# Kernel optimization log

Measured on AMD Instinct MI355X. Metric: run time of the kernel, lower is better.

## Reference

```python
import jax, jax.numpy as jnp
import numpy as np

N_NODES, N_EDGES, BATCH_SIZE = 8192, 65536, 64
N_S, NG, MAX_R = 16, 32, 10.0
SQRT3 = float(np.sqrt(3.0))


def _mlp2(h, w1, b1, w2, b2):
    return jax.nn.relu(h @ w1 + b1) @ w2 + b2


def _mlp3(h, w1, b1, w2, b2, w3, b3):
    h = jax.nn.relu(h @ w1 + b1)
    h = jax.nn.relu(h @ w2 + b2)
    return h @ w3 + b3


def _scatter_mean(vals, idx, n):
    s = jax.ops.segment_sum(vals, idx, num_segments=n)
    c = jax.ops.segment_sum(jnp.ones(vals.shape[:1], vals.dtype), idx, num_segments=n)
    return s / jnp.maximum(c, 1.0)[:, None]


def _forward_molecule(x, pos, src, dst, batch, params):
    (ne_w1, ne_b1, ne_w2, ne_b2, ee_w1, ee_b1, ee_w2, ee_b2,
     c0_w1, c0_b1, c0_w2, c0_b2, c1_w1, c1_b1, c1_w2, c1_b2,
     sn_w1, sn_b1, sn_w2, sn_b2, sn_w3, sn_b3,
     se_w1, se_b1, se_w2, se_b2, se_w3, se_b3) = params
    n = x.shape[0]
    evec = pos[dst] - pos[src]                       # [E,3]
    dist = jnp.sqrt(jnp.sum(evec * evec, -1) + 1e-12)
    mu = jnp.linspace(0.0, MAX_R, NG)
    coeff = -0.5 / (MAX_R / (NG - 1)) ** 2           # GaussianSmearing
    edge_attr = jnp.exp(coeff * (dist[:, None] - mu) ** 2)     # [E,NG]
    sh1 = SQRT3 * evec / dist[:, None]               # l=1 SH, component norm; l=0 part == 1

    h = _mlp2(x, ne_w1, ne_b1, ne_w2, ne_b2)         # node embedding [N,16]
    eemb = _mlp2(edge_attr, ee_w1, ee_b1, ee_w2, ee_b2)        # edge embedding [E,16]

    # ---- conv 0: 16x0e (x) 0e+1o -> 16x0e+16x1o, per-edge TP weights ----
    ea = jnp.concatenate([eemb, h[dst, :N_S], h[src, :N_S]], -1)   # [E,48]
    w = _mlp2(ea, c0_w1, c0_b1, c0_w2, c0_b2)                      # [E,512]
    E = w.shape[0]
    w00 = w[:, :256].reshape(E, 16, 16)    # 0e x 0e -> 0e
    w01 = w[:, 256:].reshape(E, 16, 16)    # 0e x 1o -> 1o
    xs = h[src]
    o0 = 0.25 * jnp.einsum('eu,euw->ew', xs, w00)        # path weight 1/sqrt(16)
    o1 = 0.25 * jnp.einsum('eu,em,euw->ewm', xs, sh1, w01)
    tp = jnp.concatenate([o0, o1.reshape(E, 48)], -1)
    up = _scatter_mean(tp, dst, n)                       # [N,64]
    h = jnp.pad(h, ((0, 0), (0, up.shape[1] - h.shape[1]))) + up

    # ---- conv 1: 16x0e+16x1o (x) 0e+1o -> 16x0e+16x1o+16x1e ----
    ea = jnp.concatenate([eemb, h[dst, :N_S], h[src, :N_S]], -1)
    w = _mlp2(ea, c1_w1, c1_b1, c1_w2, c1_b2)                      # [E,1280]
    wA, wB, wC, wD, wE = (w[:, i * 256:(i + 1) * 256].reshape(E, 16, 16) for i in range(5))
    x0s = h[src, :16]
    x1s = h[src, 16:64].reshape(E, 16, 3)
    pw = 1.0 / float(np.sqrt(32.0))        # two fan-16 paths into 0e and into 1o
    o0 = pw * (jnp.einsum('eu,euw->ew', x0s, wA)
               + jnp.einsum('eui,ei,euw->ew', x1s, sh1, wD) / SQRT3)  # CG(1,1,0)=delta/sqrt3
    o1o = pw * (jnp.einsum('eu,em,euw->ewm', x0s, sh1, wB)
                + jnp.einsum('eum,euw->ewm', x1s, wC))
    cr = jnp.cross(x1s, sh1[:, None, :])                              # CG(1,1,1)=eps/sqrt2
    o1e = (0.25 / float(np.sqrt(2.0))) * jnp.einsum('euk,euw->ewk', cr, wE)
    tp = jnp.concatenate([o0, o1o.reshape(E, 48), o1e.reshape(E, 48)], -1)
    up = _scatter_mean(tp, dst, n)                       # [N,112]
    h = jnp.pad(h, ((0, 0), (0, up.shape[1] - h.shape[1]))) + up

    xf = h[:, :N_S]                                      # n_conv_layers < 3 branch
    s_nodes = _mlp3(xf, sn_w1, sn_b1, sn_w2, sn_b2, sn_w3, sn_b3)   # [N,1]
    s_edges = _mlp3(jnp.concatenate([edge_attr, xf[src], xf[dst]], -1),
                    se_w1, se_b1, se_w2, se_b2, se_w3, se_b3)       # [E,1]
    # edge_in_score=True -> edge and node scatter_add into per-molecule score
    return (jax.ops.segment_sum(s_edges, batch[src], num_segments=BATCH_SIZE)
            + jax.ops.segment_sum(s_nodes, batch, num_segments=BATCH_SIZE))


def setup_inputs() -> dict:
    ks = iter(jax.random.split(jax.random.key(0), 64))

    def nrm(shape, scale=1.0):
        return scale * jax.random.normal(next(ks), shape, jnp.float32)

    def lin(fi, fo):
        return nrm((fi, fo), 1.0 / float(np.sqrt(fi)))

    def z(n):
        return jnp.zeros((n,), jnp.float32)

    inp = {}
    for tag in ('r', 'p'):
        inp[f'x_{tag}'] = nrm((N_NODES, 32))
        inp[f'pos_{tag}'] = 2.0 * jax.random.normal(next(ks), (N_NODES, 3), jnp.float32)
        s = jax.random.randint(next(ks), (N_EDGES,), 0, N_NODES)
        o = jax.random.randint(next(ks), (N_EDGES,), 1, N_NODES)   # no self loops
        inp[f'edge_index_{tag}'] = jnp.stack([s, (s + o) % N_NODES]).astype(jnp.int32)
        inp[f'batch_{tag}'] = jnp.sort(jax.random.randint(next(ks), (N_NODES,), 0, BATCH_SIZE)).astype(jnp.int32)
    inp['ne_w1'] = lin(32, 16); inp['ne_b1'] = z(16); inp['ne_w2'] = lin(16, 16); inp['ne_b2'] = z(16)
    inp['ee_w1'] = lin(32, 16); inp['ee_b1'] = z(16); inp['ee_w2'] = lin(16, 16); inp['ee_b2'] = z(16)
    inp['c0_w1'] = lin(48, 48); inp['c0_b1'] = z(48); inp['c0_w2'] = lin(48, 512); inp['c0_b2'] = z(512)
    inp['c1_w1'] = lin(48, 48); inp['c1_b1'] = z(48); inp['c1_w2'] = lin(48, 1280); inp['c1_b2'] = z(1280)
    inp['sn_w1'] = lin(16, 32); inp['sn_b1'] = z(32); inp['sn_w2'] = lin(32, 16); inp['sn_b2'] = z(16)
    inp['sn_w3'] = lin(16, 1); inp['sn_b3'] = z(1)
    inp['se_w1'] = lin(64, 16); inp['se_b1'] = z(16); inp['se_w2'] = lin(16, 16); inp['se_b2'] = z(16)
    inp['se_w3'] = lin(16, 1); inp['se_b3'] = z(1)
    return inp


def reference(x_r, pos_r, edge_index_r, batch_r, x_p, pos_p, edge_index_p, batch_p,
              ne_w1, ne_b1, ne_w2, ne_b2, ee_w1, ee_b1, ee_w2, ee_b2,
              c0_w1, c0_b1, c0_w2, c0_b2, c1_w1, c1_b1, c1_w2, c1_b2,
              sn_w1, sn_b1, sn_w2, sn_b2, sn_w3, sn_b3,
              se_w1, se_b1, se_w2, se_b2, se_w3, se_b3):
    params = (ne_w1, ne_b1, ne_w2, ne_b2, ee_w1, ee_b1, ee_w2, ee_b2,
              c0_w1, c0_b1, c0_w2, c0_b2, c1_w1, c1_b1, c1_w2, c1_b2,
              sn_w1, sn_b1, sn_w2, sn_b2, sn_w3, sn_b3,
              se_w1, se_b1, se_w2, se_b2, se_w3, se_b3)
    e_r = _forward_molecule(x_r, pos_r, edge_index_r[0], edge_index_r[1], batch_r, params)
    e_p = _forward_molecule(x_p, pos_p, edge_index_p[0], edge_index_p[1], batch_p, params)
    return e_p - e_r   # reaction energy [BATCH_SIZE, 1]
```

## Files before the change

### kernel.cpp

```cpp
#include <hip/hip_runtime.h>
#include <math.h>

#define NN 8192
#define NE 65536
#define SQRT3F 1.7320508075688772f
#define INV_SQRT3F 0.5773502691896258f
#define PW 0.17677669529663687f
#define GSTEP (10.0f/31.0f)
#define GCOEFF (-0.5f/(GSTEP*GSTEP))

typedef _Float16 f16;
typedef f16 f16x2 __attribute__((ext_vector_type(2)));
typedef f16 f16x4 __attribute__((ext_vector_type(4)));
typedef f16 f16x8 __attribute__((ext_vector_type(8)));
typedef float f32x4 __attribute__((ext_vector_type(4)));

#define MFMA(acc, a, b) acc = __builtin_amdgcn_mfma_f32_16x16x32_f16(a, b, acc, 0, 0, 0)

__global__ __launch_bounds__(256) void k_pre(const float* __restrict__ c0w1, const float* __restrict__ c0b1,
                                             const float* __restrict__ c1w1, const float* __restrict__ c1b1,
                                             const float* __restrict__ c0w2, const float* __restrict__ c0b2,
                                             const float* __restrict__ c1w2, const float* __restrict__ c1b2,
                                             f16* __restrict__ w1c0, f16* __restrict__ w1c1,
                                             f16* __restrict__ w2t0, f16* __restrict__ w2t1,
                                             const float* __restrict__ xr, const float* __restrict__ xp,
                                             float* __restrict__ h16f, f16* __restrict__ h16_16,
                                             const float* __restrict__ nw1, const float* __restrict__ nb1,
                                             const float* __restrict__ nw2, const float* __restrict__ nb2,
                                             const int* __restrict__ eir, const int* __restrict__ eip,
                                             const float* __restrict__ posr, const float* __restrict__ posp,
                                             float* __restrict__ sh1d, f16* __restrict__ eemb16,
                                             int* __restrict__ cnt,
                                             const float* __restrict__ ew1, const float* __restrict__ eb1,
                                             const float* __restrict__ ew2, const float* __restrict__ eb2) {
    int b = blockIdx.x;
    int tid = threadIdx.x;
    if (b < 320) {
        int idx = b * 256 + tid;
        if (idx >= 1280 * 64) return;
        int n = idx >> 6, h = idx & 63;
        w2t1[idx] = (f16)((h < 48) ? c1w2[h * 1280 + n] : (h == 48 ? c1b2[n] : 0.f));
        if (n < 512) w2t0[idx] = (f16)((h < 48) ? c0w2[h * 512 + n] : (h == 48 ? c0b2[n] : 0.f));
        if (n < 48) {
            w1c0[idx] = (f16)((h < 48) ? c0w1[h * 48 + n] : (h == 48 ? c0b1[n] : 0.f));
            w1c1[idx] = (f16)((h < 48) ? c1w1[h * 48 + n] : (h == 48 ? c1b1[n] : 0.f));
        }
    } else if (b < 384) {
        int bb = b - 320;
        int mol = bb >> 5;
        const float* x = mol ? xp : xr;
        float* hf = h16f + (size_t)mol * NN * 16;
        f16* h16o = h16_16 + (size_t)mol * NN * 16;
        int v = (bb & 31) * 256 + tid;
        float xi[32];
#pragma unroll
        for (int i = 0; i < 32; i++) xi[i] = x[v * 32 + i];
        float a[16];
#pragma unroll
        for (int j = 0; j < 16; j++) a[j] = nb1[j];
#pragma unroll
        for (int i = 0; i < 32; i++)
#pragma unroll
            for (int j = 0; j < 16; j++) a[j] = fmaf(xi[i], nw1[i * 16 + j], a[j]);
#pragma unroll
        for (int j = 0; j < 16; j++) a[j] = fmaxf(a[j], 0.f);
        float o[16];
#pragma unroll
        for (int j = 0; j < 16; j++) o[j] = nb2[j];
#pragma unroll
        for (int i = 0; i < 16; i++)
#pragma unroll
            for (int j = 0; j < 16; j++) o[j] = fmaf(a[i], nw2[i * 16 + j], o[j]);
#pragma unroll
        for (int j = 0; j < 16; j++) { hf[v * 16 + j] = o[j]; h16o[v * 16 + j] = (f16)o[j]; }
    } else {
        int bb = b - 384;
        int mol = bb >> 8;
        const int* ei = mol ? eip : eir;
        const float* pos = mol ? posp : posr;
        float* sh_ = sh1d + (size_t)mol * NE * 4;
        f16* em_ = eemb16 + (size_t)mol * NE * 16;
        int* cn_ = cnt + mol * NN;
        int e = (bb & 255) * 256 + tid;
        int s = ei[e], d = ei[NE + e];
        float ex = pos[d * 3 + 0] - pos[s * 3 + 0];
        float ey = pos[d * 3 + 1] - pos[s * 3 + 1];
        float ez = pos[d * 3 + 2] - pos[s * 3 + 2];
        float dist = sqrtf(ex * ex + ey * ey + ez * ez + 1e-12f);
        float inv = SQRT3F / dist;
        sh_[e * 4 + 0] = ex * inv;
        sh_[e * 4 + 1] = ey * inv;
        sh_[e * 4 + 2] = ez * inv;
        sh_[e * 4 + 3] = dist;
        float g[32];
#pragma unroll
        for (int i = 0; i < 32; i++) {
            float t = dist - (float)i * GSTEP;
            g[i] = __expf(GCOEFF * t * t);
        }
        float a[16];
#pragma unroll
        for (int j = 0; j < 16; j++) a[j] = eb1[j];
#pragma unroll
        for (int i = 0; i < 32; i++)
#pragma unroll
            for (int j = 0; j < 16; j++) a[j] = fmaf(g[i], ew1[i * 16 + j], a[j]);
#pragma unroll
        for (int j = 0; j < 16; j++) a[j] = fmaxf(a[j], 0.f);
        float o[16];
#pragma unroll
        for (int j = 0; j < 16; j++) o[j] = eb2[j];
#pragma unroll
        for (int i = 0; i < 16; i++)
#pragma unroll
            for (int j = 0; j < 16; j++) o[j] = fmaf(a[i], ew2[i * 16 + j], o[j]);
#pragma unroll
        for (int j = 0; j < 16; j++) em_[e * 16 + j] = (f16)o[j];
        atomicAdd(&cn_[d], 1);
    }
}

__global__ __launch_bounds__(256) void k_scan(int* __restrict__ cnt, int* __restrict__ rowptr,
                                              float* __restrict__ out) {
    __shared__ int part[256];
    int mol = blockIdx.x;
    int* c = cnt + mol * NN;
    int* rp = rowptr + mol * (NN + 1);
    int t = threadIdx.x;
    int base = t * (NN / 256);
    int s = 0;
#pragma unroll
    for (int i = 0; i < NN / 256; i++) s += c[base + i];
    part[t] = s;
    __syncthreads();
    if (t == 0) {
        int run = 0;
        for (int i = 0; i < 256; i++) { int v = part[i]; part[i] = run; run += v; }
    }
    __syncthreads();
    int run = part[t];
    for (int i = 0; i < NN / 256; i++) {
        int cv = c[base + i];
        rp[base + i] = run;
        run += cv;
        c[base + i] = 0;
    }
    if (t == 255) rp[NN] = run;
    if (mol == 0 && t < 64) out[t] = 0.f;
}

__global__ __launch_bounds__(256) void k_fill(const int* __restrict__ eir, const int* __restrict__ eip,
                                              const int* __restrict__ rowptr, int* __restrict__ cnt,
                                              int* __restrict__ eord) {
    int mol = blockIdx.y;
    const int* ei = mol ? eip : eir;
    int e = blockIdx.x * 256 + threadIdx.x;
    int d = ei[NE + e];
    int pos = atomicAdd(&cnt[mol * NN + d], 1);
    eord[mol * NE + rowptr[mol * (NN + 1) + d] + pos] = e;
}

__global__ __launch_bounds__(128) void k_conv0(const int* __restrict__ eir, const int* __restrict__ eip,
                                               const int* __restrict__ eord,
                                               const f16* __restrict__ eemb16, const f16* __restrict__ h16_16,
                                               const float* __restrict__ sh1d,
                                               const f16* __restrict__ w1h, const f16* __restrict__ w2h,
                                               f16* __restrict__ tp0) {
    __shared__ __align__(16) f16 ea[256 * 72];
    __shared__ __align__(16) f16 sc0[256 * 24];
    __shared__ __align__(16) float4 shs[256];
    int mol = blockIdx.y;
    const int* ei = mol ? eip : eir;
    const int* eo = eord + mol * NE;
    const f16* em_ = eemb16 + (size_t)mol * NE * 16;
    const f16* h16_ = h16_16 + (size_t)mol * NN * 16;
    const float* sh_ = sh1d + (size_t)mol * NE * 4;
    f16* tp_ = tp0 + (size_t)mol * NE * 64;
    int tid = threadIdx.x;
    int e0 = blockIdx.x * 256;
#pragma unroll
    for (int ii = 0; ii < 2; ii++) {
        int er = tid * 2 + ii;
        int le = eo[e0 + er];
        int s = ei[le], d = ei[NE + le];
        char* row = (char*)ea + er * 144;
        const f16x8* pe = (const f16x8*)(em_ + (size_t)le * 16);
        ((f16x8*)row)[0] = pe[0]; ((f16x8*)row)[1] = pe[1];
        const f16x8* pd = (const f16x8*)(h16_ + (size_t)d * 16);
        ((f16x8*)row)[2] = pd[0]; ((f16x8*)row)[3] = pd[1];
        const f16x8* ps = (const f16x8*)(h16_ + (size_t)s * 16);
        f16x8 sv0 = ps[0], sv1 = ps[1];
        ((f16x8*)row)[4] = sv0; ((f16x8*)row)[5] = sv1;
        f16x8 z = {}; f16x8 o = {}; o[0] = (f16)1.0f;
        ((f16x8*)row)[6] = o; ((f16x8*)row)[7] = z; ((f16x8*)row)[8] = z;
        char* srow = (char*)sc0 + er * 48;
        *(f16x8*)srow = sv0;
        *(f16x8*)(srow + 16) = sv1;
        shs[er] = *(const float4*)(sh_ + (size_t)le * 4);
    }
    int wv = tid >> 6, l = tid & 63;
    int koff = (l >> 4) * 16;
    int voffB = (l & 15) * 128 + koff;
    int rbase = wv * 128;
#pragma unroll
    for (int t = 0; t < 8; t++) {
        int arow = rbase + t * 16 + (l & 15);
        f16x8 a0 = *(const f16x8*)((const char*)ea + arow * 144 + koff);
        f16x8 a1 = *(const f16x8*)((const char*)ea + arow * 144 + koff + 64);
#pragma unroll
        for (int nt = 0; nt < 3; nt++) {
            f32x4 hacc = {0.f, 0.f, 0.f, 0.f};
            const char* hb = (const char*)w1h + nt * 2048 + voffB;
            MFMA(hacc, a0, *(const f16x8*)(hb));
            MFMA(hacc, a1, *(const f16x8*)(hb + 64));
#pragma unroll
            for (int r = 0; r < 4; r++) {
                int rr = rbase + t * 16 + (l >> 4) * 4 + r;
                ea[rr * 72 + nt * 16 + (l & 15)] = (f16)fmaxf(hacc[r], 0.f);
            }
        }
    }
    f16x8 ha0[8], ha1[8];
#pragma unroll
    for (int t = 0; t < 8; t++) {
        int arow = rbase + t * 16 + (l & 15);
        ha0[t] = *(const f16x8*)((const char*)ea + arow * 144 + koff);
        ha1[t] = *(const f16x8*)((const char*)ea + arow * 144 + koff + 64);
    }
    f32x4 accA[8] = {}, accB[8] = {};
    const char* wB = (const char*)w2h + voffB;
    f16x8 cA0 = *(const f16x8*)(wB), cA1 = *(const f16x8*)(wB + 64);
    f16x8 cB0 = *(const f16x8*)(wB + 32768), cB1 = *(const f16x8*)(wB + 32768 + 64);
#pragma unroll 4
    for (int u = 0; u < 16; ++u) {
        int un = (u < 15) ? u + 1 : 15;
        const char* Hb = wB + un * 2048;
        f16x8 nA0 = *(const f16x8*)(Hb), nA1 = *(const f16x8*)(Hb + 64);
        f16x8 nB0 = *(const f16x8*)(Hb + 32768), nB1 = *(const f16x8*)(Hb + 32768 + 64);
#pragma unroll
        for (int t = 0; t < 8; t++) {
            f16 s = *(const f16*)((const char*)sc0 + (rbase + t * 16 + (l & 15)) * 48 + u * 2);
            f16x8 x0 = ha0[t] * s, x1 = ha1[t] * s;
            MFMA(accA[t], x0, cA0); MFMA(accA[t], x1, cA1);
            MFMA(accB[t], x0, cB0); MFMA(accB[t], x1, cB1);
        }
        cA0 = nA0; cA1 = nA1; cB0 = nB0; cB1 = nB1;
    }
    int w = l & 15;
#pragma unroll
    for (int t = 0; t < 8; t++)
#pragma unroll
        for (int r = 0; r < 4; r++) {
            int ro = rbase + t * 16 + (l >> 4) * 4 + r;
            int i = e0 + ro;
            float4 shv = shs[ro];
            f16* tpp = tp_ + (size_t)i * 64;
            float tb = 0.25f * accB[t][r];
            tpp[w] = (f16)(0.25f * accA[t][r]);
            tpp[16 + w] = (f16)(tb * shv.x);
            tpp[32 + w] = (f16)(tb * shv.y);
            tpp[48 + w] = (f16)(tb * shv.z);
        }
}

__global__ __launch_bounds__(256) void k_up0g(const float* __restrict__ h16f, const f16* __restrict__ tp0,
                                              const int* __restrict__ rowptr,
                                              float* __restrict__ h64f, f16* __restrict__ h64_16) {
    int mol = blockIdx.y;
    const float* h_ = h16f + (size_t)mol * NN * 16;
    const f16* tp = tp0 + (size_t)mol * NE * 64;
    const int* rp = rowptr + mol * (NN + 1);
    float* o_ = h64f + (size_t)mol * NN * 64;
    f16* o16_ = h64_16 + (size_t)mol * NN * 16;
    int tid = threadIdx.x;
    int v = blockIdx.x * 64 + (tid >> 2), q = tid & 3;
    int r0 = rp[v], r1 = rp[v + 1];
    float acc[16];
#pragma unroll
    for (int j = 0; j < 16; j++) acc[j] = 0.f;
    for (int i = r0; i < r1; i++) {
        const f16* src = tp + (size_t)i * 64 + q * 16;
        f16x8 v0 = *(const f16x8*)src;
        f16x8 v1 = *(const f16x8*)(src + 8);
#pragma unroll
        for (int j = 0; j < 8; j++) { acc[j] += (float)v0[j]; acc[8 + j] += (float)v1[j]; }
    }
    float rc = 1.0f / fmaxf((float)(r1 - r0), 1.0f);
    if (q == 0) {
#pragma unroll
        for (int w = 0; w < 16; w++) {
            float val = fmaf(acc[w], rc, h_[(size_t)v * 16 + w]);
            o_[(size_t)v * 64 + w] = val;
            o16_[(size_t)v * 16 + w] = (f16)val;
        }
    } else {
#pragma unroll
        for (int w = 0; w < 16; w++) o_[(size_t)v * 64 + 16 + 3 * w + (q - 1)] = acc[w] * rc;
    }
}

__global__ __launch_bounds__(128) void k_conv1(const int* __restrict__ eir, const int* __restrict__ eip,
                                               const int* __restrict__ eord,
                                               const f16* __restrict__ eemb16, const f16* __restrict__ h64_16,
                                               const float* __restrict__ h64f, const float* __restrict__ sh1d,
                                               const f16* __restrict__ w1h, const f16* __restrict__ w2h,
                                               f16* __restrict__ tp1) {
    __shared__ __align__(16) f16 ea[256 * 72];
    __shared__ __align__(16) f16 sc1[256 * 36];
    int mol = blockIdx.y;
    const int* ei = mol ? eip : eir;
    const int* eo = eord + mol * NE;
    const f16* em_ = eemb16 + (size_t)mol * NE * 16;
    const f16* h16_ = h64_16 + (size_t)mol * NN * 16;
    const float* hf_ = h64f + (size_t)mol * NN * 64;
    const float* sh_ = sh1d + (size_t)mol * NE * 4;
    f16* tp_ = tp1 + (size_t)mol * NE * 16;
    int tid = threadIdx.x;
    int e0 = blockIdx.x * 256;
#pragma unroll
    for (int ii = 0; ii < 2; ii++) {
        int er = tid * 2 + ii;
        int le = eo[e0 + er];
        int s = ei[le], d = ei[NE + le];
        char* row = (char*)ea + er * 144;
        const f16x8* pe = (const f16x8*)(em_ + (size_t)le * 16);
        ((f16x8*)row)[0] = pe[0]; ((f16x8*)row)[1] = pe[1];
        const f16x8* pd = (const f16x8*)(h16_ + (size_t)d * 16);
        ((f16x8*)row)[2] = pd[0]; ((f16x8*)row)[3] = pd[1];
        const f16x8* ps = (const f16x8*)(h16_ + (size_t)s * 16);
        ((f16x8*)row)[4] = ps[0]; ((f16x8*)row)[5] = ps[1];
        f16x8 z = {}; f16x8 o = {}; o[0] = (f16)1.0f;
        ((f16x8*)row)[6] = o; ((f16x8*)row)[7] = z; ((f16x8*)row)[8] = z;
        float4 shv = *(const float4*)(sh_ + (size_t)le * 4);
        const float* hfs = hf_ + (size_t)s * 64;
        float xu[16];
#pragma unroll
        for (int g = 0; g < 4; g++) {
            float4 v4 = *(const float4*)(hfs + g * 4);
            xu[g * 4 + 0] = v4.x; xu[g * 4 + 1] = v4.y; xu[g * 4 + 2] = v4.z; xu[g * 4 + 3] = v4.w;
        }
        float x1v[48];
#pragma unroll
        for (int g = 0; g < 12; g++) {
            float4 v4 = *(const float4*)(hfs + 16 + g * 4);
            x1v[g * 4 + 0] = v4.x; x1v[g * 4 + 1] = v4.y; x1v[g * 4 + 2] = v4.z; x1v[g * 4 + 3] = v4.w;
        }
        char* srow = (char*)sc1 + er * 72;
#pragma unroll
        for (int g = 0; g < 4; g++) {
            f16x8 pk;
#pragma unroll
            for (int k2 = 0; k2 < 4; k2++) {
                int k = g * 4 + k2;
                float du = (x1v[k * 3] * shv.x + x1v[k * 3 + 1] * shv.y + x1v[k * 3 + 2] * shv.z) * INV_SQRT3F;
                pk[k2 * 2 + 0] = (f16)xu[k];
                pk[k2 * 2 + 1] = (f16)du;
            }
            *(f16x8*)(srow + g * 16) = pk;
        }
    }
    int wv = tid >> 6, l = tid & 63;
    int koff = (l >> 4) * 16;
    int voffB = (l & 15) * 128 + koff;
    int rbase = wv * 128;
#pragma unroll
    for (int t = 0; t < 8; t++) {
        int arow = rbase + t * 16 + (l & 15);
        f16x8 a0 = *(const f16x8*)((const char*)ea + arow * 144 + koff);
        f16x8 a1 = *(const f16x8*)((const char*)ea + arow * 144 + koff + 64);
#pragma unroll
        for (int nt = 0; nt < 3; nt++) {
            f32x4 hacc = {0.f, 0.f, 0.f, 0.f};
            const char* hb = (const char*)w1h + nt * 2048 + voffB;
            MFMA(hacc, a0, *(const f16x8*)(hb));
            MFMA(hacc, a1, *(const f16x8*)(hb + 64));
#pragma unroll
            for (int r = 0; r < 4; r++) {
                int rr = rbase + t * 16 + (l >> 4) * 4 + r;
                ea[rr * 72 + nt * 16 + (l & 15)] = (f16)fmaxf(hacc[r], 0.f);
            }
        }
    }
    f16x8 ha0[8], ha1[8];
#pragma unroll
    for (int t = 0; t < 8; t++) {
        int arow = rbase + t * 16 + (l & 15);
        ha0[t] = *(const f16x8*)((const char*)ea + arow * 144 + koff);
        ha1[t] = *(const f16x8*)((const char*)ea + arow * 144 + koff + 64);
    }
    f32x4 accA[8] = {};
    const char* wB = (const char*)w2h + voffB;
    f16x8 cA0 = *(const f16x8*)(wB), cA1 = *(const f16x8*)(wB + 64);
    f16x8 cD0 = *(const f16x8*)(wB + 98304), cD1 = *(const f16x8*)(wB + 98304 + 64);
#pragma unroll 4
    for (int u = 0; u < 16; ++u) {
        int un = (u < 15) ? u + 1 : 15;
        const char* Hb = wB + un * 2048;
        f16x8 nA0 = *(const f16x8*)(Hb), nA1 = *(const f16x8*)(Hb + 64);
        f16x8 nD0 = *(const f16x8*)(Hb + 98304), nD1 = *(const f16x8*)(Hb + 98304 + 64);
#pragma unroll
        for (int t = 0; t < 8; t++) {
            f16x2 sp = *(const f16x2*)((const char*)sc1 + (rbase + t * 16 + (l & 15)) * 72 + u * 4);
            f16x8 x0 = ha0[t] * sp[0], x1 = ha1[t] * sp[0];
            MFMA(accA[t], x0, cA0); MFMA(accA[t], x1, cA1);
            x0 = ha0[t] * sp[1]; x1 = ha1[t] * sp[1];
            MFMA(accA[t], x0, cD0); MFMA(accA[t], x1, cD1);
        }
        cA0 = nA0; cA1 = nA1; cD0 = nD0; cD1 = nD1;
    }
    int w = l & 15;
#pragma unroll
    for (int t = 0; t < 8; t++)
#pragma unroll
        for (int r = 0; r < 4; r++) {
            int i = e0 + rbase + t * 16 + (l >> 4) * 4 + r;
            tp_[(size_t)i * 16 + w] = (f16)(PW * accA[t][r]);
        }
}

__global__ __launch_bounds__(256) void k_xfg(const float* __restrict__ h64f, const f16* __restrict__ tp1,
                                             const int* __restrict__ rowptr,
                                             float* __restrict__ xf,
                                             const int* __restrict__ batchr, const int* __restrict__ batchp,
                                             const float* __restrict__ w1, const float* __restrict__ b1,
                                             const float* __restrict__ w2, const float* __restrict__ b2,
                                             const float* __restrict__ w3, const float* __restrict__ b3,
                                             float* __restrict__ out) {
    __shared__ float xfs[64][17];
    __shared__ float buck[64];
    int tid = threadIdx.x;
    if (tid < 64) buck[tid] = 0.f;
    int mol = blockIdx.y;
    float sign = mol ? 1.f : -1.f;
    const int* batch = mol ? batchp : batchr;
    const float* h_ = h64f + (size_t)mol * NN * 64;
    const f16* tp = tp1 + (size_t)mol * NE * 16;
    const int* rp = rowptr + mol * (NN + 1);
    float* xf_ = xf + (size_t)mol * NN * 16;
    int v = blockIdx.x * 64 + (tid >> 2), q = tid & 3;
    int r0 = rp[v], r1 = rp[v + 1];
    float a0 = 0.f, a1 = 0.f, a2 = 0.f, a3 = 0.f;
    for (int i = r0; i < r1; i++) {
        f16x4 t4 = *(const f16x4*)(tp + (size_t)i * 16 + q * 4);
        a0 += (float)t4[0]; a1 += (float)t4[1]; a2 += (float)t4[2]; a3 += (float)t4[3];
    }
    float rc = 1.0f / fmaxf((float)(r1 - r0), 1.0f);
    float4 hv = *(const float4*)(h_ + (size_t)v * 64 + q * 4);
    float4 xv4;
    xv4.x = fmaf(a0, rc, hv.x); xv4.y = fmaf(a1, rc, hv.y);
    xv4.z = fmaf(a2, rc, hv.z); xv4.w = fmaf(a3, rc, hv.w);
    xfs[tid >> 2][q * 4 + 0] = xv4.x; xfs[tid >> 2][q * 4 + 1] = xv4.y;
    xfs[tid >> 2][q * 4 + 2] = xv4.z; xfs[tid >> 2][q * 4 + 3] = xv4.w;
    *(float4*)(xf_ + (size_t)v * 16 + q * 4) = xv4;
    __syncthreads();
    if (tid < 64) {
        int v2 = blockIdx.x * 64 + tid;
        float xv[16];
#pragma unroll
        for (int c = 0; c < 16; c++) xv[c] = xfs[tid][c];
        float aa[32];
#pragma unroll
        for (int j = 0; j < 32; j++) aa[j] = b1[j];
#pragma unroll
        for (int i = 0; i < 16; i++)
#pragma unroll
            for (int j = 0; j < 32; j++) aa[j] = fmaf(xv[i], w1[i * 32 + j], aa[j]);
#pragma unroll
        for (int j = 0; j < 32; j++) aa[j] = fmaxf(aa[j], 0.f);
        float bb[16];
#pragma unroll
        for (int j = 0; j < 16; j++) bb[j] = b2[j];
#pragma unroll
        for (int i = 0; i < 32; i++)
#pragma unroll
            for (int j = 0; j < 16; j++) bb[j] = fmaf(aa[i], w2[i * 16 + j], bb[j]);
#pragma unroll
        for (int j = 0; j < 16; j++) bb[j] = fmaxf(bb[j], 0.f);
        float val = b3[0];
#pragma unroll
        for (int i = 0; i < 16; i++) val = fmaf(bb[i], w3[i], val);
        atomicAdd(&buck[batch[v2]], val);
    }
    __syncthreads();
    if (tid < 64) atomicAdd(&out[tid], sign * buck[tid]);
}

__global__ __launch_bounds__(256) void k_sedge(const int* __restrict__ eir, const int* __restrict__ eip,
                                               const int* __restrict__ batchr, const int* __restrict__ batchp,
                                               const float* __restrict__ sh1d, const float* __restrict__ xf,
                                               const float* __restrict__ w1, const float* __restrict__ b1,
                                               const float* __restrict__ w2, const float* __restrict__ b2,
                                               const float* __restrict__ w3, const float* __restrict__ b3,
                                               float* __restrict__ out) {
    __shared__ float buck[64];
    int tid = threadIdx.x;
    if (tid < 64) buck[tid] = 0.f;
    __syncthreads();
    int mol = blockIdx.y;
    float sign = mol ? 1.f : -1.f;
    const int* ei = mol ? eip : eir;
    const int* batch = mol ? batchp : batchr;
    const float* sh_ = sh1d + (size_t)mol * NE * 4;
    const float* xf_ = xf + (size_t)mol * NN * 16;
    int e = blockIdx.x * 256 + tid;
    int s = ei[e], d = ei[NE + e];
    float dist = sh_[e * 4 + 3];
    float in[64];
#pragma unroll
    for (int i = 0; i < 32; i++) {
        float t = dist - (float)i * GSTEP;
        in[i] = __expf(GCOEFF * t * t);
    }
#pragma unroll
    for (int i = 0; i < 16; i++) in[32 + i] = xf_[s * 16 + i];
#pragma unroll
    for (int i = 0; i < 16; i++) in[48 + i] = xf_[d * 16 + i];
    float a[16];
#pragma unroll
    for (int j = 0; j < 16; j++) a[j] = b1[j];
#pragma unroll
    for (int i = 0; i < 64; i++)
#pragma unroll
        for (int j = 0; j < 16; j++) a[j] = fmaf(in[i], w1[i * 16 + j], a[j]);
#pragma unroll
    for (int j = 0; j < 16; j++) a[j] = fmaxf(a[j], 0.f);
    float bb[16];
#pragma unroll
    for (int j = 0; j < 16; j++) bb[j] = b2[j];
#pragma unroll
    for (int i = 0; i < 16; i++)
#pragma unroll
        for (int j = 0; j < 16; j++) bb[j] = fmaf(a[i], w2[i * 16 + j], bb[j]);
#pragma unroll
    for (int j = 0; j < 16; j++) bb[j] = fmaxf(bb[j], 0.f);
    float val = b3[0];
#pragma unroll
    for (int i = 0; i < 16; i++) val = fmaf(bb[i], w3[i], val);
    atomicAdd(&buck[batch[s]], val);
    __syncthreads();
    if (tid < 64) atomicAdd(&out[tid], sign * buck[tid]);
}

extern "C" void kernel_launch(void* const* d_in, const int* in_sizes, int n_in,
                              void* d_out, int out_size, void* d_ws, size_t ws_size,
                              hipStream_t stream) {
    const float* x_r = (const float*)d_in[0];
    const float* pos_r = (const float*)d_in[1];
    const int* ei_r = (const int*)d_in[2];
    const int* batch_r = (const int*)d_in[3];
    const float* x_p = (const float*)d_in[4];
    const float* pos_p = (const float*)d_in[5];
    const int* ei_p = (const int*)d_in[6];
    const int* batch_p = (const int*)d_in[7];
    const float* ne_w1 = (const float*)d_in[8];
    const float* ne_b1 = (const float*)d_in[9];
    const float* ne_w2 = (const float*)d_in[10];
    const float* ne_b2 = (const float*)d_in[11];
    const float* ee_w1 = (const float*)d_in[12];
    const float* ee_b1 = (const float*)d_in[13];
    const float* ee_w2 = (const float*)d_in[14];
    const float* ee_b2 = (const float*)d_in[15];
    const float* c0_w1 = (const float*)d_in[16];
    const float* c0_b1 = (const float*)d_in[17];
    const float* c0_w2 = (const float*)d_in[18];
    const float* c0_b2 = (const float*)d_in[19];
    const float* c1_w1 = (const float*)d_in[20];
    const float* c1_b1 = (const float*)d_in[21];
    const float* c1_w2 = (const float*)d_in[22];
    const float* c1_b2 = (const float*)d_in[23];
    const float* sn_w1 = (const float*)d_in[24];
    const float* sn_b1 = (const float*)d_in[25];
    const float* sn_w2 = (const float*)d_in[26];
    const float* sn_b2 = (const float*)d_in[27];
    const float* sn_w3 = (const float*)d_in[28];
    const float* sn_b3 = (const float*)d_in[29];
    const float* se_w1 = (const float*)d_in[30];
    const float* se_b1 = (const float*)d_in[31];
    const float* se_w2 = (const float*)d_in[32];
    const float* se_b2 = (const float*)d_in[33];
    const float* se_w3 = (const float*)d_in[34];
    const float* se_b3 = (const float*)d_in[35];
    float* out = (float*)d_out;

    char* p = (char*)d_ws;
    auto alloc = [&](size_t bytes) { char* r = p; p += (bytes + 255) & ~(size_t)255; return r; };
    f16* w2t1 = (f16*)alloc(1280 * 64 * 2);
    f16* w2t0 = (f16*)alloc(512 * 64 * 2);
    f16* w1c0 = (f16*)alloc(48 * 64 * 2);
    f16* w1c1 = (f16*)alloc(48 * 64 * 2);
    f16* eemb16 = (f16*)alloc((size_t)2 * NE * 16 * 2);
    f16* h16_16 = (f16*)alloc((size_t)2 * NN * 16 * 2);
    f16* h64_16 = (f16*)alloc((size_t)2 * NN * 16 * 2);
    float* h16f = (float*)alloc((size_t)2 * NN * 16 * 4);
    float* sh1d = (float*)alloc((size_t)2 * NE * 4 * 4);
    int* cntI = (int*)alloc((size_t)2 * NN * 4);
    int* rowptr = (int*)alloc((size_t)2 * (NN + 1) * 4);
    int* eord = (int*)alloc((size_t)2 * NE * 4);
    f16* tp0 = (f16*)alloc((size_t)2 * NE * 64 * 2);
    f16* tp1 = tp0;
    float* h64f = (float*)alloc((size_t)2 * NN * 64 * 4);
    float* xf = (float*)alloc((size_t)2 * NN * 16 * 4);
    (void)ws_size; (void)n_in; (void)in_sizes; (void)out_size;

    hipMemsetAsync(cntI, 0, (size_t)2 * NN * 4, stream);

    dim3 blk256(256, 1, 1), blk128(128, 1, 1);
    dim3 ge(NE / 256, 2, 1);
    dim3 gc(NE / 256, 2, 1);

    k_pre<<<dim3(896, 1, 1), blk256, 0, stream>>>(c0_w1, c0_b1, c1_w1, c1_b1, c0_w2, c0_b2, c1_w2, c1_b2,
                                                  w1c0, w1c1, w2t0, w2t1,
                                                  x_r, x_p, h16f, h16_16, ne_w1, ne_b1, ne_w2, ne_b2,
                                                  ei_r, ei_p, pos_r, pos_p, sh1d, eemb16, cntI,
                                                  ee_w1, ee_b1, ee_w2, ee_b2);
    k_scan<<<dim3(2, 1, 1), blk256, 0, stream>>>(cntI, rowptr, out);
    k_fill<<<ge, blk256, 0, stream>>>(ei_r, ei_p, rowptr, cntI, eord);
    k_conv0<<<gc, blk128, 0, stream>>>(ei_r, ei_p, eord, eemb16, h16_16, sh1d, w1c0, w2t0, tp0);
    k_up0g<<<dim3(NN / 64, 2, 1), blk256, 0, stream>>>(h16f, tp0, rowptr, h64f, h64_16);
    k_conv1<<<gc, blk128, 0, stream>>>(ei_r, ei_p, eord, eemb16, h64_16, h64f, sh1d, w1c1, w2t1, tp1);
    k_xfg<<<dim3(NN / 64, 2, 1), blk256, 0, stream>>>(h64f, tp1, rowptr, xf, batch_r, batch_p,
                                                      sn_w1, sn_b1, sn_w2, sn_b2, sn_w3, sn_b3, out);
    k_sedge<<<ge, blk256, 0, stream>>>(ei_r, ei_p, batch_r, batch_p, sh1d, xf,
                                       se_w1, se_b1, se_w2, se_b2, se_w3, se_b3, out);
}
```

Baseline: 147.8 us.

## Fuse all stages into one persistent kernel with software grid barriers

Replaces the eight separate kernel launches (preprocess, scan, fill, conv0, update, conv1, node readout, edge readout) with a single persistent kernel of 512 blocks. Stages are separated by an atomic-counter grid barrier, and the barrier counter is zeroed by the existing memset. The aim is to remove per-launch overhead and inter-kernel gaps. In exchange, all 512 blocks must be co-resident for the barrier to be safe, the barrier adds spin and fence cost, and the scan stage runs on only 2 blocks while the rest wait.

Result: slower. 571.5 us (+286.7%).

```diff
diff --git a/kernel.cpp b/kernel.cpp
--- a/kernel.cpp
+++ b/kernel.cpp
@@ -3,6 +3,7 @@
 
 #define NN 8192
 #define NE 65536
+#define NB 512
 #define SQRT3F 1.7320508075688772f
 #define INV_SQRT3F 0.5773502691896258f
 #define PW 0.17677669529663687f
@@ -17,609 +18,603 @@
 
 #define MFMA(acc, a, b) acc = __builtin_amdgcn_mfma_f32_16x16x32_f16(a, b, acc, 0, 0, 0)
 
-__global__ __launch_bounds__(256) void k_pre(const float* __restrict__ c0w1, const float* __restrict__ c0b1,
-                                             const float* __restrict__ c1w1, const float* __restrict__ c1b1,
-                                             const float* __restrict__ c0w2, const float* __restrict__ c0b2,
-                                             const float* __restrict__ c1w2, const float* __restrict__ c1b2,
-                                             f16* __restrict__ w1c0, f16* __restrict__ w1c1,
-                                             f16* __restrict__ w2t0, f16* __restrict__ w2t1,
-                                             const float* __restrict__ xr, const float* __restrict__ xp,
-                                             float* __restrict__ h16f, f16* __restrict__ h16_16,
-                                             const float* __restrict__ nw1, const float* __restrict__ nb1,
-                                             const float* __restrict__ nw2, const float* __restrict__ nb2,
-                                             const int* __restrict__ eir, const int* __restrict__ eip,
-                                             const float* __restrict__ posr, const float* __restrict__ posp,
-                                             float* __restrict__ sh1d, f16* __restrict__ eemb16,
-                                             int* __restrict__ cnt,
-                                             const float* __restrict__ ew1, const float* __restrict__ eb1,
-                                             const float* __restrict__ ew2, const float* __restrict__ eb2) {
-    int b = blockIdx.x;
-    int tid = threadIdx.x;
-    if (b < 320) {
-        int idx = b * 256 + tid;
-        if (idx >= 1280 * 64) return;
-        int n = idx >> 6, h = idx & 63;
-        w2t1[idx] = (f16)((h < 48) ? c1w2[h * 1280 + n] : (h == 48 ? c1b2[n] : 0.f));
-        if (n < 512) w2t0[idx] = (f16)((h < 48) ? c0w2[h * 512 + n] : (h == 48 ? c0b2[n] : 0.f));
-        if (n < 48) {
-            w1c0[idx] = (f16)((h < 48) ? c0w1[h * 48 + n] : (h == 48 ? c0b1[n] : 0.f));
-            w1c1[idx] = (f16)((h < 48) ? c1w1[h * 48 + n] : (h == 48 ? c1b1[n] : 0.f));
-        }
-    } else if (b < 384) {
-        int bb = b - 320;
-        int mol = bb >> 5;
-        const float* x = mol ? xp : xr;
-        float* hf = h16f + (size_t)mol * NN * 16;
-        f16* h16o = h16_16 + (size_t)mol * NN * 16;
-        int v = (bb & 31) * 256 + tid;
+struct KP {
+    const float *c0w1, *c0b1, *c1w1, *c1b1, *c0w2, *c0b2, *c1w2, *c1b2;
+    f16 *w1c0, *w1c1, *w2t0, *w2t1;
+    const float *xr, *xp;
+    float* h16f; f16* h16_16;
+    const float *nw1, *nb1, *nw2, *nb2;
+    const int *eir, *eip;
+    const float *posr, *posp;
+    float* sh1d; f16* eemb16; int* cnt;
+    const float *ew1, *eb1, *ew2, *eb2;
+    int* rowptr; int* eord;
+    f16* tp0; f16* tp1;
+    float* h64f; f16* h64_16;
+    float* xf;
+    const int *batchr, *batchp;
+    const float *snw1, *snb1, *snw2, *snb2, *snw3, *snb3;
+    const float *sew1, *seb1, *sew2, *seb2, *sew3, *seb3;
+    float* out;
+    int* bar;
+};
+
+__device__ __forceinline__ void gridbar(int* bar, int phase) {
+    __syncthreads();
+    if (threadIdx.x == 0) {
+        __threadfence();
+        atomicAdd(bar, 1);
+        int target = (phase + 1) * NB;
+        int it = 0;
+        while (atomicAdd(bar, 0) < target && it < (1 << 22)) {
+            ++it;
+            __builtin_amdgcn_s_sleep(8);
+        }
+    }
+    __syncthreads();
+    __threadfence();
+}
+
+__global__ __launch_bounds__(128) void k_mega(KP P) {
+    __shared__ __align__(16) char smem[55296];
+    int bid = blockIdx.x, tid = threadIdx.x;
+    int gtid = bid * 128 + tid;
+
+    if (gtid < 64) P.out[gtid] = 0.f;
+    {
+#pragma unroll
+        for (int it = 0; it < 2; ++it) {
+            int idx = gtid + it * 65536;
+            if (idx < 1280 * 64) {
+                int n = idx >> 6, h = idx & 63;
+                P.w2t1[idx] = (f16)((h < 48) ? P.c1w2[h * 1280 + n] : (h == 48 ? P.c1b2[n] : 0.f));
+                if (n < 512) P.w2t0[idx] = (f16)((h < 48) ? P.c0w2[h * 512 + n] : (h == 48 ? P.c0b2[n] : 0.f));
+                if (n < 48) {
+                    P.w1c0[idx] = (f16)((h < 48) ? P.c0w1[h * 48 + n] : (h == 48 ? P.c0b1[n] : 0.f));
+                    P.w1c1[idx] = (f16)((h < 48) ? P.c1w1[h * 48 + n] : (h == 48 ? P.c1b1[n] : 0.f));
+                }
+            }
+        }
+    }
+    if (gtid < 2 * NN) {
+        int mol = gtid >> 13;
+        int v = gtid & (NN - 1);
+        const float* x = mol ? P.xp : P.xr;
+        float* hf = P.h16f + (size_t)mol * NN * 16;
+        f16* h16o = P.h16_16 + (size_t)mol * NN * 16;
         float xi[32];
 #pragma unroll
         for (int i = 0; i < 32; i++) xi[i] = x[v * 32 + i];
         float a[16];
 #pragma unroll
-        for (int j = 0; j < 16; j++) a[j] = nb1[j];
+        for (int j = 0; j < 16; j++) a[j] = P.nb1[j];
 #pragma unroll
         for (int i = 0; i < 32; i++)
 #pragma unroll
-            for (int j = 0; j < 16; j++) a[j] = fmaf(xi[i], nw1[i * 16 + j], a[j]);
+            for (int j = 0; j < 16; j++) a[j] = fmaf(xi[i], P.nw1[i * 16 + j], a[j]);
 #pragma unroll
         for (int j = 0; j < 16; j++) a[j] = fmaxf(a[j], 0.f);
         float o[16];
 #pragma unroll
-        for (int j = 0; j < 16; j++) o[j] = nb2[j];
+        for (int j = 0; j < 16; j++) o[j] = P.nb2[j];
 #pragma unroll
         for (int i = 0; i < 16; i++)
 #pragma unroll
-            for (int j = 0; j < 16; j++) o[j] = fmaf(a[i], nw2[i * 16 + j], o[j]);
+            for (int j = 0; j < 16; j++) o[j] = fmaf(a[i], P.nw2[i * 16 + j], o[j]);
 #pragma unroll
         for (int j = 0; j < 16; j++) { hf[v * 16 + j] = o[j]; h16o[v * 16 + j] = (f16)o[j]; }
-    } else {
-        int bb = b - 384;
-        int mol = bb >> 8;
-        const int* ei = mol ? eip : eir;
-        const float* pos = mol ? posp : posr;
-        float* sh_ = sh1d + (size_t)mol * NE * 4;
-        f16* em_ = eemb16 + (size_t)mol * NE * 16;
-        int* cn_ = cnt + mol * NN;
-        int e = (bb & 255) * 256 + tid;
-        int s = ei[e], d = ei[NE + e];
-        float ex = pos[d * 3 + 0] - pos[s * 3 + 0];
-        float ey = pos[d * 3 + 1] - pos[s * 3 + 1];
-        float ez = pos[d * 3 + 2] - pos[s * 3 + 2];
-        float dist = sqrtf(ex * ex + ey * ey + ez * ez + 1e-12f);
-        float inv = SQRT3F / dist;
-        sh_[e * 4 + 0] = ex * inv;
-        sh_[e * 4 + 1] = ey * inv;
-        sh_[e * 4 + 2] = ez * inv;
-        sh_[e * 4 + 3] = dist;
-        float g[32];
-#pragma unroll
-        for (int i = 0; i < 32; i++) {
-            float t = dist - (float)i * GSTEP;
-            g[i] = __expf(GCOEFF * t * t);
-        }
-        float a[16];
-#pragma unroll
-        for (int j = 0; j < 16; j++) a[j] = eb1[j];
-#pragma unroll
-        for (int i = 0; i < 32; i++)
-#pragma unroll
-            for (int j = 0; j < 16; j++) a[j] = fmaf(g[i], ew1[i * 16 + j], a[j]);
-#pragma unroll
-        for (int j = 0; j < 16; j++) a[j] = fmaxf(a[j], 0.f);
-        float o[16];
-#pragma unroll
-        for (int j = 0; j < 16; j++) o[j] = eb2[j];
-#pragma unroll
-        for (int i = 0; i < 16; i++)
-#pragma unroll
-            for (int j = 0; j < 16; j++) o[j] = fmaf(a[i], ew2[i * 16 + j], o[j]);
-#pragma unroll
-        for (int j = 0; j < 16; j++) em_[e * 16 + j] = (f16)o[j];
-        atomicAdd(&cn_[d], 1);
-    }
-}
-
-__global__ __launch_bounds__(256) void k_scan(int* __restrict__ cnt, int* __restrict__ rowptr,
-                                              float* __restrict__ out) {
-    __shared__ int part[256];
-    int mol = blockIdx.x;
-    int* c = cnt + mol * NN;
-    int* rp = rowptr + mol * (NN + 1);
-    int t = threadIdx.x;
-    int base = t * (NN / 256);
-    int s = 0;
-#pragma unroll
-    for (int i = 0; i < NN / 256; i++) s += c[base + i];
-    part[t] = s;
-    __syncthreads();
-    if (t == 0) {
-        int run = 0;
-        for (int i = 0; i < 256; i++) { int v = part[i]; part[i] = run; run += v; }
-    }
-    __syncthreads();
-    int run = part[t];
-    for (int i = 0; i < NN / 256; i++) {
-        int cv = c[base + i];
-        rp[base + i] = run;
-        run += cv;
-        c[base + i] = 0;
-    }
-    if (t == 255) rp[NN] = run;
-    if (mol == 0 && t < 64) out[t] = 0.f;
-}
-
-__global__ __launch_bounds__(256) void k_fill(const int* __restrict__ eir, const int* __restrict__ eip,
-                                              const int* __restrict__ rowptr, int* __restrict__ cnt,
-                                              int* __restrict__ eord) {
-    int mol = blockIdx.y;
-    const int* ei = mol ? eip : eir;
-    int e = blockIdx.x * 256 + threadIdx.x;
-    int d = ei[NE + e];
-    int pos = atomicAdd(&cnt[mol * NN + d], 1);
-    eord[mol * NE + rowptr[mol * (NN + 1) + d] + pos] = e;
-}
-
-__global__ __launch_bounds__(128) void k_conv0(const int* __restrict__ eir, const int* __restrict__ eip,
-                                               const int* __restrict__ eord,
-                                               const f16* __restrict__ eemb16, const f16* __restrict__ h16_16,
-                                               const float* __restrict__ sh1d,
-                                               const f16* __restrict__ w1h, const f16* __restrict__ w2h,
-                                               f16* __restrict__ tp0) {
-    __shared__ __align__(16) f16 ea[256 * 72];
-    __shared__ __align__(16) f16 sc0[256 * 24];
-    __shared__ __align__(16) float4 shs[256];
-    int mol = blockIdx.y;
-    const int* ei = mol ? eip : eir;
-    const int* eo = eord + mol * NE;
-    const f16* em_ = eemb16 + (size_t)mol * NE * 16;
-    const f16* h16_ = h16_16 + (size_t)mol * NN * 16;
-    const float* sh_ = sh1d + (size_t)mol * NE * 4;
-    f16* tp_ = tp0 + (size_t)mol * NE * 64;
-    int tid = threadIdx.x;
-    int e0 = blockIdx.x * 256;
-#pragma unroll
-    for (int ii = 0; ii < 2; ii++) {
-        int er = tid * 2 + ii;
-        int le = eo[e0 + er];
-        int s = ei[le], d = ei[NE + le];
-        char* row = (char*)ea + er * 144;
-        const f16x8* pe = (const f16x8*)(em_ + (size_t)le * 16);
-        ((f16x8*)row)[0] = pe[0]; ((f16x8*)row)[1] = pe[1];
-        const f16x8* pd = (const f16x8*)(h16_ + (size_t)d * 16);
-        ((f16x8*)row)[2] = pd[0]; ((f16x8*)row)[3] = pd[1];
-        const f16x8* ps = (const f16x8*)(h16_ + (size_t)s * 16);
-        f16x8 sv0 = ps[0], sv1 = ps[1];
-        ((f16x8*)row)[4] = sv0; ((f16x8*)row)[5] = sv1;
-        f16x8 z = {}; f16x8 o = {}; o[0] = (f16)1.0f;
-        ((f16x8*)row)[6] = o; ((f16x8*)row)[7] = z; ((f16x8*)row)[8] = z;
-        char* srow = (char*)sc0 + er * 48;
-        *(f16x8*)srow = sv0;
-        *(f16x8*)(srow + 16) = sv1;
-        shs[er] = *(const float4*)(sh_ + (size_t)le * 4);
-    }
-    int wv = tid >> 6, l = tid & 63;
-    int koff = (l >> 4) * 16;
-    int voffB = (l & 15) * 128 + koff;
-    int rbase = wv * 128;
-#pragma unroll
-    for (int t = 0; t < 8; t++) {
-        int arow = rbase + t * 16 + (l & 15);
-        f16x8 a0 = *(const f16x8*)((const char*)ea + arow * 144 + koff);
-        f16x8 a1 = *(const f16x8*)((const char*)ea + arow * 144 + koff + 64);
-#pragma unroll
-        for (int nt = 0; nt < 3; nt++) {
-            f32x4 hacc = {0.f, 0.f, 0.f, 0.f};
-            const char* hb = (const char*)w1h + nt * 2048 + voffB;
-            MFMA(hacc, a0, *(const f16x8*)(hb));
-            MFMA(hacc, a1, *(const f16x8*)(hb + 64));
+    }
+    {
+#pragma unroll 1
+        for (int mol = 0; mol < 2; ++mol) {
+            const int* ei = mol ? P.eip : P.eir;
+            const float* pos = mol ? P.posp : P.posr;
+            float* sh_ = P.sh1d + (size_t)mol * NE * 4;
+            f16* em_ = P.eemb16 + (size_t)mol * NE * 16;
+            int* cn_ = P.cnt + mol * NN;
+            int e = gtid;
+            int s = ei[e], d = ei[NE + e];
+            float ex = pos[d * 3 + 0] - pos[s * 3 + 0];
+            float ey = pos[d * 3 + 1] - pos[s * 3 + 1];
+            float ez = pos[d * 3 + 2] - pos[s * 3 + 2];
+            float dist = sqrtf(ex * ex + ey * ey + ez * ez + 1e-12f);
+            float inv = SQRT3F / dist;
+            sh_[e * 4 + 0] = ex * inv;
+            sh_[e * 4 + 1] = ey * inv;
+            sh_[e * 4 + 2] = ez * inv;
+            sh_[e * 4 + 3] = dist;
+            float g[32];
+#pragma unroll
+            for (int i = 0; i < 32; i++) {
+                float t = dist - (float)i * GSTEP;
+                g[i] = __expf(GCOEFF * t * t);
+            }
+            float a[16];
+#pragma unroll
+            for (int j = 0; j < 16; j++) a[j] = P.eb1[j];
+#pragma unroll
+            for (int i = 0; i < 32; i++)
+#pragma unroll
+                for (int j = 0; j < 16; j++) a[j] = fmaf(g[i], P.ew1[i * 16 + j], a[j]);
+#pragma unroll
+            for (int j = 0; j < 16; j++) a[j] = fmaxf(a[j], 0.f);
+            float o[16];
+#pragma unroll
+            for (int j = 0; j < 16; j++) o[j] = P.eb2[j];
+#pragma unroll
+            for (int i = 0; i < 16; i++)
+#pragma unroll
+                for (int j = 0; j < 16; j++) o[j] = fmaf(a[i], P.ew2[i * 16 + j], o[j]);
+#pragma unroll
+            for (int j = 0; j < 16; j++) em_[e * 16 + j] = (f16)o[j];
+            atomicAdd(&cn_[d], 1);
+        }
+    }
+    gridbar(P.bar, 0);
+
+    if (bid < 2) {
+        int* part = (int*)smem;
+        int mol = bid;
+        int* c = P.cnt + mol * NN;
+        int* rp = P.rowptr + mol * (NN + 1);
+        int base = tid * (NN / 128);
+        int s = 0;
+#pragma unroll
+        for (int i = 0; i < NN / 128; i++) s += c[base + i];
+        part[tid] = s;
+        __syncthreads();
+        if (tid == 0) {
+            int run = 0;
+            for (int i = 0; i < 128; i++) { int v = part[i]; part[i] = run; run += v; }
+        }
+        __syncthreads();
+        int run = part[tid];
+        for (int i = 0; i < NN / 128; i++) {
+            int cv = c[base + i];
+            rp[base + i] = run;
+            run += cv;
+            c[base + i] = 0;
+        }
+        if (tid == 127) rp[NN] = run;
+    }
+    gridbar(P.bar, 1);
+
+#pragma unroll 1
+    for (int mol = 0; mol < 2; ++mol) {
+        const int* ei = mol ? P.eip : P.eir;
+        int e = gtid;
+        int d = ei[NE + e];
+        int pos = atomicAdd(&P.cnt[mol * NN + d], 1);
+        P.eord[mol * NE + P.rowptr[mol * (NN + 1) + d] + pos] = e;
+    }
+    gridbar(P.bar, 2);
+
+    {
+        f16* ea = (f16*)smem;
+        f16* sc0 = (f16*)(smem + 36864);
+        float4* shs = (float4*)(smem + 49152);
+        int mol = bid >> 8;
+        int cb = bid & 255;
+        const int* ei = mol ? P.eip : P.eir;
+        const int* eo = P.eord + mol * NE;
+        const f16* em_ = P.eemb16 + (size_t)mol * NE * 16;
+        const f16* h16_ = P.h16_16 + (size_t)mol * NN * 16;
+        const float* sh_ = P.sh1d + (size_t)mol * NE * 4;
+        f16* tp_ = P.tp0 + (size_t)mol * NE * 64;
+        int e0 = cb * 256;
+#pragma unroll
+        for (int ii = 0; ii < 2; ii++) {
+            int er = tid * 2 + ii;
+            int le = eo[e0 + er];
+            int s = ei[le], d = ei[NE + le];
+            char* row = smem + er * 144;
+            const f16x8* pe = (const f16x8*)(em_ + (size_t)le * 16);
+            ((f16x8*)row)[0] = pe[0]; ((f16x8*)row)[1] = pe[1];
+            const f16x8* pd = (const f16x8*)(h16_ + (size_t)d * 16);
+            ((f16x8*)row)[2] = pd[0]; ((f16x8*)row)[3] = pd[1];
+            const f16x8* ps = (const f16x8*)(h16_ + (size_t)s * 16);
+            f16x8 sv0 = ps[0], sv1 = ps[1];
+            ((f16x8*)row)[4] = sv0; ((f16x8*)row)[5] = sv1;
+            f16x8 z = {}; f16x8 o = {}; o[0] = (f16)1.0f;
+            ((f16x8*)row)[6] = o; ((f16x8*)row)[7] = z; ((f16x8*)row)[8] = z;
+            char* srow = (char*)sc0 + er * 48;
+            *(f16x8*)srow = sv0;
+            *(f16x8*)(srow + 16) = sv1;
+            shs[er] = *(const float4*)(sh_ + (size_t)le * 4);
+        }
+        __syncthreads();
+        int wv = tid >> 6, l = tid & 63;
+        int koff = (l >> 4) * 16;
+        int voffB = (l & 15) * 128 + koff;
+        int rbase = wv * 128;
+#pragma unroll
+        for (int t = 0; t < 8; t++) {
+            int arow = rbase + t * 16 + (l & 15);
+            f16x8 a0 = *(const f16x8*)((const char*)ea + arow * 144 + koff);
+            f16x8 a1 = *(const f16x8*)((const char*)ea + arow * 144 + koff + 64);
+#pragma unroll
+            for (int nt = 0; nt < 3; nt++) {
+                f32x4 hacc = {0.f, 0.f, 0.f, 0.f};
+                const char* hb = (const char*)P.w1c0 + nt * 2048 + voffB;
+                MFMA(hacc, a0, *(const f16x8*)(hb));
+                MFMA(hacc, a1, *(const f16x8*)(hb + 64));
+#pragma unroll
+                for (int r = 0; r < 4; r++) {
+                    int rr = rbase + t * 16 + (l >> 4) * 4 + r;
+                    ea[rr * 72 + nt * 16 + (l & 15)] = (f16)fmaxf(hacc[r], 0.f);
+                }
+            }
+        }
+        f16x8 ha0[8], ha1[8];
+#pragma unroll
+        for (int t = 0; t < 8; t++) {
+            int arow = rbase + t * 16 + (l & 15);
+            ha0[t] = *(const f16x8*)((const char*)ea + arow * 144 + koff);
+            ha1[t] = *(const f16x8*)((const char*)ea + arow * 144 + koff + 64);
+        }
+        f32x4 accA[8] = {}, accB[8] = {};
+        const char* wB = (const char*)P.w2t0 + voffB;
+        f16x8 cA0 = *(const f16x8*)(wB), cA1 = *(const f16x8*)(wB + 64);
+        f16x8 cB0 = *(const f16x8*)(wB + 32768), cB1 = *(const f16x8*)(wB + 32768 + 64);
+#pragma unroll 4
+        for (int u = 0; u < 16; ++u) {
+            int un = (u < 15) ? u + 1 : 15;
+            const char* Hb = wB + un * 2048;
+            f16x8 nA0 = *(const f16x8*)(Hb), nA1 = *(const f16x8*)(Hb + 64);
+            f16x8 nB0 = *(const f16x8*)(Hb + 32768), nB1 = *(const f16x8*)(Hb + 32768 + 64);
+#pragma unroll
+            for (int t = 0; t < 8; t++) {
+                f16 s = *(const f16*)((const char*)sc0 + (rbase + t * 16 + (l & 15)) * 48 + u * 2);
+                f16x8 x0 = ha0[t] * s, x1 = ha1[t] * s;
+                MFMA(accA[t], x0, cA0); MFMA(accA[t], x1, cA1);
+                MFMA(accB[t], x0, cB0); MFMA(accB[t], x1, cB1);
+            }
+            cA0 = nA0; cA1 = nA1; cB0 = nB0; cB1 = nB1;
+        }
+        int w = l & 15;
+#pragma unroll
+        for (int t = 0; t < 8; t++)
 #pragma unroll
             for (int r = 0; r < 4; r++) {
-                int rr = rbase + t * 16 + (l >> 4) * 4 + r;
-                ea[rr * 72 + nt * 16 + (l & 15)] = (f16)fmaxf(hacc[r], 0.f);
-            }
-        }
-    }
-    f16x8 ha0[8], ha1[8];
-#pragma unroll
-    for (int t = 0; t < 8; t++) {
-        int arow = rbase + t * 16 + (l & 15);
-        ha0[t] = *(const f16x8*)((const char*)ea + arow * 144 + koff);
-        ha1[t] = *(const f16x8*)((const char*)ea + arow * 144 + koff + 64);
-    }
-    f32x4 accA[8] = {}, accB[8] = {};
-    const char* wB = (const char*)w2h + voffB;
-    f16x8 cA0 = *(const f16x8*)(wB), cA1 = *(const f16x8*)(wB + 64);
-    f16x8 cB0 = *(const f16x8*)(wB + 32768), cB1 = *(const f16x8*)(wB + 32768 + 64);
+                int ro = rbase + t * 16 + (l >> 4) * 4 + r;
+                int i = e0 + ro;
+                float4 shv = shs[ro];
+                f16* tpp = tp_ + (size_t)i * 64;
+                float tb = 0.25f * accB[t][r];
+                tpp[w] = (f16)(0.25f * accA[t][r]);
+                tpp[16 + w] = (f16)(tb * shv.x);
+                tpp[32 + w] = (f16)(tb * shv.y);
+                tpp[48 + w] = (f16)(tb * shv.z);
+            }
+    }
+    gridbar(P.bar, 3);
+
+    {
+        int mol = bid >> 8;
+        const float* h_ = P.h16f + (size_t)mol * NN * 16;
+        const f16* tp = P.tp0 + (size_t)mol * NE * 64;
+        const int* rp = P.rowptr + mol * (NN + 1);
+        float* o_ = P.h64f + (size_t)mol * NN * 64;
+        f16* o16_ = P.h64_16 + (size_t)mol * NN * 16;
+        int v = (bid & 255) * 32 + (tid >> 2), q = tid & 3;
+        int r0 = rp[v], r1 = rp[v + 1];
+        float acc[16];
+#pragma unroll
+        for (int j = 0; j < 16; j++) acc[j] = 0.f;
+        for (int i = r0; i < r1; i++) {
+            const f16* src = tp + (size_t)i * 64 + q * 16;
+            f16x8 v0 = *(const f16x8*)src;
+            f16x8 v1 = *(const f16x8*)(src + 8);
+#pragma unroll
+            for (int j = 0; j < 8; j++) { acc[j] += (float)v0[j]; acc[8 + j] += (float)v1[j]; }
+        }
+        float rc = 1.0f / fmaxf((float)(r1 - r0), 1.0f);
+        if (q == 0) {
+#pragma unroll
+            for (int w = 0; w < 16; w++) {
+                float val = fmaf(acc[w], rc, h_[(size_t)v * 16 + w]);
+                o_[(size_t)v * 64 + w] = val;
+                o16_[(size_t)v * 16 + w] = (f16)val;
+            }
+        } else {
+#pragma unroll
+            for (int w = 0; w < 16; w++) o_[(size_t)v * 64 + 16 + 3 * w + (q - 1)] = acc[w] * rc;
+        }
+    }
+    gridbar(P.bar, 4);
+
+    {
+        f16* ea = (f16*)smem;
+        f16* sc1 = (f16*)(smem + 36864);
+        int mol = bid >> 8;
+        int cb = bid & 255;
+        const int* ei = mol ? P.eip : P.eir;
+        const int* eo = P.eord + mol * NE;
+        const f16* em_ = P.eemb16 + (size_t)mol * NE * 16;
+        const f16* h16_ = P.h64_16 + (size_t)mol * NN * 16;
+        const float* hf_ = P.h64f + (size_t)mol * NN * 64;
+        const float* sh_ = P.sh1d + (size_t)mol * NE * 4;
+        f16* tp_ = P.tp1 + (size_t)mol * NE * 16;
+        int e0 = cb * 256;
+#pragma unroll
+        for (int ii = 0; ii < 2; ii++) {
+            int er = tid * 2 + ii;
+            int le = eo[e0 + er];
+            int s = ei[le], d = ei[NE + le];
+            char* row = smem + er * 144;
+            const f16x8* pe = (const f16x8*)(em_ + (size_t)le * 16);
+            ((f16x8*)row)[0] = pe[0]; ((f16x8*)row)[1] = pe[1];
+            const f16x8* pd = (const f16x8*)(h16_ + (size_t)d * 16);
+            ((f16x8*)row)[2] = pd[0]; ((f16x8*)row)[3] = pd[1];
+            const f16x8* ps = (const f16x8*)(h16_ + (size_t)s * 16);
+            ((f16x8*)row)[4] = ps[0]; ((f16x8*)row)[5] = ps[1];
+            f16x8 z = {}; f16x8 o = {}; o[0] = (f16)1.0f;
+            ((f16x8*)row)[6] = o; ((f16x8*)row)[7] = z; ((f16x8*)row)[8] = z;
+            float4 shv = *(const float4*)(sh_ + (size_t)le * 4);
+            const float* hfs = hf_ + (size_t)s * 64;
+            float xu[16];
+#pragma unroll
+            for (int g = 0; g < 4; g++) {
+                float4 v4 = *(const float4*)(hfs + g * 4);
+                xu[g * 4 + 0] = v4.x; xu[g * 4 + 1] = v4.y; xu[g * 4 + 2] = v4.z; xu[g * 4 + 3] = v4.w;
+            }
+            float x1v[48];
+#pragma unroll
+            for (int g = 0; g < 12; g++) {
+                float4 v4 = *(const float4*)(hfs + 16 + g * 4);
+                x1v[g * 4 + 0] = v4.x; x1v[g * 4 + 1] = v4.y; x1v[g * 4 + 2] = v4.z; x1v[g * 4 + 3] = v4.w;
+            }
+            char* srow = (char*)sc1 + er * 72;
+#pragma unroll
+            for (int g = 0; g < 4; g++) {
+                f16x8 pk;
+#pragma unroll
+                for (int k2 = 0; k2 < 4; k2++) {
+                    int k = g * 4 + k2;
+                    float du = (x1v[k * 3] * shv.x + x1v[k * 3 + 1] * shv.y + x1v[k * 3 + 2] * shv.z) * INV_SQRT3F;
+                    pk[k2 * 2 + 0] = (f16)xu[k];
+                    pk[k2 * 2 + 1] = (f16)du;
+                }
+                *(f16x8*)(srow + g * 16) = pk;
+            }
+        }
+        __syncthreads();
+        int wv = tid >> 6, l = tid & 63;
+        int koff = (l >> 4) * 16;
+        int voffB = (l & 15) * 128 + koff;
+        int rbase = wv * 128;
+#pragma unroll
+        for (int t = 0; t < 8; t++) {
+            int arow = rbase + t * 16 + (l & 15);
+            f16x8 a0 = *(const f16x8*)((const char*)ea + arow * 144 + koff);
+            f16x8 a1 = *(const f16x8*)((const char*)ea + arow * 144 + koff + 64);
+#pragma unroll
+            for (int nt = 0; nt < 3; nt++) {
+                f32x4 hacc = {0.f, 0.f, 0.f, 0.f};
+                const char* hb = (const char*)P.w1c1 + nt * 2048 + voffB;
+                MFMA(hacc, a0, *(const f16x8*)(hb));
+                MFMA(hacc, a1, *(const f16x8*)(hb + 64));
+#pragma unroll
+                for (int r = 0; r < 4; r++) {
+                    int rr = rbase + t * 16 + (l >> 4) * 4 + r;
+                    ea[rr * 72 + nt * 16 + (l & 15)] = (f16)fmaxf(hacc[r], 0.f);
+                }
+            }
+        }
+        f16x8 ha0[8], ha1[8];
+#pragma unroll
+        for (int t = 0; t < 8; t++) {
+            int arow = rbase + t * 16 + (l & 15);
+            ha0[t] = *(const f16x8*)((const char*)ea + arow * 144 + koff);
+            ha1[t] = *(const f16x8*)((const char*)ea + arow * 144 + koff + 64);
+        }
+        f32x4 accA[8] = {};
+        const char* wB = (const char*)P.w2t1 + voffB;
+        f16x8 cA0 = *(const f16x8*)(wB), cA1 = *(const f16x8*)(wB + 64);
+        f16x8 cD0 = *(const f16x8*)(wB + 98304), cD1 = *(const f16x8*)(wB + 98304 + 64);
 #pragma unroll 4
-    for (int u = 0; u < 16; ++u) {
-        int un = (u < 15) ? u + 1 : 15;
-        const char* Hb = wB + un * 2048;
-        f16x8 nA0 = *(const f16x8*)(Hb), nA1 = *(const f16x8*)(Hb + 64);
-        f16x8 nB0 = *(const f16x8*)(Hb + 32768), nB1 = *(const f16x8*)(Hb + 32768 + 64);
-#pragma unroll
-        for (int t = 0; t < 8; t++) {
-            f16 s = *(const f16*)((const char*)sc0 + (rbase + t * 16 + (l & 15)) * 48 + u * 2);
-            f16x8 x0 = ha0[t] * s, x1 = ha1[t] * s;
-            MFMA(accA[t], x0, cA0); MFMA(accA[t], x1, cA1);
-            MFMA(accB[t], x0, cB0); MFMA(accB[t], x1, cB1);
-        }
-        cA0 = nA0; cA1 = nA1; cB0 = nB0; cB1 = nB1;
-    }
-    int w = l & 15;
-#pragma unroll
-    for (int t = 0; t < 8; t++)
-#pragma unroll
-        for (int r = 0; r < 4; r++) {
-            int ro = rbase + t * 16 + (l >> 4) * 4 + r;
-            int i = e0 + ro;
-            float4 shv = shs[ro];
-            f16* tpp = tp_ + (size_t)i * 64;
-            float tb = 0.25f * accB[t][r];
-            tpp[w] = (f16)(0.25f * accA[t][r]);
-            tpp[16 + w] = (f16)(tb * shv.x);
-            tpp[32 + w] = (f16)(tb * shv.y);
-            tpp[48 + w] = (f16)(tb * shv.z);
-        }
-}
-
-__global__ __launch_bounds__(256) void k_up0g(const float* __restrict__ h16f, const f16* __restrict__ tp0,
-                                              const int* __restrict__ rowptr,
-                                              float* __restrict__ h64f, f16* __restrict__ h64_16) {
-    int mol = blockIdx.y;
-    const float* h_ = h16f + (size_t)mol * NN * 16;
-    const f16* tp = tp0 + (size_t)mol * NE * 64;
-    const int* rp = rowptr + mol * (NN + 1);
-    float* o_ = h64f + (size_t)mol * NN * 64;
-    f16* o16_ = h64_16 + (size_t)mol * NN * 16;
-    int tid = threadIdx.x;
-    int v = blockIdx.x * 64 + (tid >> 2), q = tid & 3;
-    int r0 = rp[v], r1 = rp[v + 1];
-    float acc[16];
-#pragma unroll
-    for (int j = 0; j < 16; j++) acc[j] = 0.f;
-    for (int i = r0; i < r1; i++) {
-        const f16* src = tp + (size_t)i * 64 + q * 16;
-        f16x8 v0 = *(const f16x8*)src;
-        f16x8 v1 = *(const f16x8*)(src + 8);
-#pragma unroll
-        for (int j = 0; j < 8; j++) { acc[j] += (float)v0[j]; acc[8 + j] += (float)v1[j]; }
-    }
-    float rc = 1.0f / fmaxf((float)(r1 - r0), 1.0f);
-    if (q == 0) {
-#pragma unroll
-        for (int w = 0; w < 16; w++) {
-            float val = fmaf(acc[w], rc, h_[(size_t)v * 16 + w]);
-            o_[(size_t)v * 64 + w] = val;
-            o16_[(size_t)v * 16 + w] = (f16)val;
-        }
-    } else {
-#pragma unroll
-        for (int w = 0; w < 16; w++) o_[(size_t)v * 64 + 16 + 3 * w + (q - 1)] = acc[w] * rc;
-    }
-}
-
-__global__ __launch_bounds__(128) void k_conv1(const int* __restrict__ eir, const int* __restrict__ eip,
-                                               const int* __restrict__ eord,
-                                               const f16* __restrict__ eemb16, const f16* __restrict__ h64_16,
-                                               const float* __restrict__ h64f, const float* __restrict__ sh1d,
-                                               const f16* __restrict__ w1h, const f16* __restrict__ w2h,
-                                               f16* __restrict__ tp1) {
-    __shared__ __align__(16) f16 ea[256 * 72];
-    __shared__ __align__(16) f16 sc1[256 * 36];
-    int mol = blockIdx.y;
-    const int* ei = mol ? eip : eir;
-    const int* eo = eord + mol * NE;
-    const f16* em_ = eemb16 + (size_t)mol * NE * 16;
-    const f16* h16_ = h64_16 + (size_t)mol * NN * 16;
-    const float* hf_ = h64f + (size_t)mol * NN * 64;
-    const float* sh_ = sh1d + (size_t)mol * NE * 4;
-    f16* tp_ = tp1 + (size_t)mol * NE * 16;
-    int tid = threadIdx.x;
-    int e0 = blockIdx.x * 256;
-#pragma unroll
-    for (int ii = 0; ii < 2; ii++) {
-        int er = tid * 2 + ii;
-        int le = eo[e0 + er];
-        int s = ei[le], d = ei[NE + le];
-        char* row = (char*)ea + er * 144;
-        const f16x8* pe = (const f16x8*)(em_ + (size_t)le * 16);
-        ((f16x8*)row)[0] = pe[0]; ((f16x8*)row)[1] = pe[1];
-        const f16x8* pd = (const f16x8*)(h16_ + (size_t)d * 16);
-        ((f16x8*)row)[2] = pd[0]; ((f16x8*)row)[3] = pd[1];
-        const f16x8* ps = (const f16x8*)(h16_ + (size_t)s * 16);
-        ((f16x8*)row)[4] = ps[0]; ((f16x8*)row)[5] = ps[1];
-        f16x8 z = {}; f16x8 o = {}; o[0] = (f16)1.0f;
-        ((f16x8*)row)[6] = o; ((f16x8*)row)[7] = z; ((f16x8*)row)[8] = z;
-        float4 shv = *(const float4*)(sh_ + (size_t)le * 4);
-        const float* hfs = hf_ + (size_t)s * 64;
-        float xu[16];
-#pragma unroll
-        for (int g = 0; g < 4; g++) {
-            float4 v4 = *(const float4*)(hfs + g * 4);
-            xu[g * 4 + 0] = v4.x; xu[g * 4 + 1] = v4.y; xu[g * 4 + 2] = v4.z; xu[g * 4 + 3] = v4.w;
-        }
-        float x1v[48];
-#pragma unroll
-        for (int g = 0; g < 12; g++) {
-            float4 v4 = *(const float4*)(hfs + 16 + g * 4);
-            x1v[g * 4 + 0] = v4.x; x1v[g * 4 + 1] = v4.y; x1v[g * 4 + 2] = v4.z; x1v[g * 4 + 3] = v4.w;
-        }
-        char* srow = (char*)sc1 + er * 72;
-#pragma unroll
-        for (int g = 0; g < 4; g++) {
-            f16x8 pk;
-#pragma unroll
-            for (int k2 = 0; k2 < 4; k2++) {
-                int k = g * 4 + k2;
-                float du = (x1v[k * 3] * shv.x + x1v[k * 3 + 1] * shv.y + x1v[k * 3 + 2] * shv.z) * INV_SQRT3F;
-                pk[k2 * 2 + 0] = (f16)xu[k];
-                pk[k2 * 2 + 1] = (f16)du;
-            }
-            *(f16x8*)(srow + g * 16) = pk;
-        }
-    }
-    int wv = tid >> 6, l = tid & 63;
-    int koff = (l >> 4) * 16;
-    int voffB = (l & 15) * 128 + koff;
-    int rbase = wv * 128;
-#pragma unroll
-    for (int t = 0; t < 8; t++) {
-        int arow = rbase + t * 16 + (l & 15);
-        f16x8 a0 = *(const f16x8*)((const char*)ea + arow * 144 + koff);
-        f16x8 a1 = *(const f16x8*)((const char*)ea + arow * 144 + koff + 64);
-#pragma unroll
-        for (int nt = 0; nt < 3; nt++) {
-            f32x4 hacc = {0.f, 0.f, 0.f, 0.f};
-            const char* hb = (const char*)w1h + nt * 2048 + voffB;
-            MFMA(hacc, a0, *(const f16x8*)(hb));
-            MFMA(hacc, a1, *(const f16x8*)(hb + 64));
+        for (int u = 0; u < 16; ++u) {
+            int un = (u < 15) ? u + 1 : 15;
+            const char* Hb = wB + un * 2048;
+            f16x8 nA0 = *(const f16x8*)(Hb), nA1 = *(const f16x8*)(Hb + 64);
+            f16x8 nD0 = *(const f16x8*)(Hb + 98304), nD1 = *(const f16x8*)(Hb + 98304 + 64);
+#pragma unroll
+            for (int t = 0; t < 8; t++) {
+                f16x2 sp = *(const f16x2*)((const char*)sc1 + (rbase + t * 16 + (l & 15)) * 72 + u * 4);
+                f16x8 x0 = ha0[t] * sp[0], x1 = ha1[t] * sp[0];
+                MFMA(accA[t], x0, cA0); MFMA(accA[t], x1, cA1);
+                x0 = ha0[t] * sp[1]; x1 = ha1[t] * sp[1];
+                MFMA(accA[t], x0, cD0); MFMA(accA[t], x1, cD1);
+            }
+            cA0 = nA0; cA1 = nA1; cD0 = nD0; cD1 = nD1;
+        }
+        int w = l & 15;
+#pragma unroll
+        for (int t = 0; t < 8; t++)
 #pragma unroll
             for (int r = 0; r < 4; r++) {
-                int rr = rbase + t * 16 + (l >> 4) * 4 + r;
-                ea[rr * 72 + nt * 16 + (l & 15)] = (f16)fmaxf(hacc[r], 0.f);
-            }
-        }
-    }
-    f16x8 ha0[8], ha1[8];
-#pragma unroll
-    for (int t = 0; t < 8; t++) {
-        int arow = rbase + t * 16 + (l & 15);
-        ha0[t] = *(const f16x8*)((const char*)ea + arow * 144 + koff);
-        ha1[t] = *(const f16x8*)((const char*)ea + arow * 144 + koff + 64);
-    }
-    f32x4 accA[8] = {};
-    const char* wB = (const char*)w2h + voffB;
-    f16x8 cA0 = *(const f16x8*)(wB), cA1 = *(const f16x8*)(wB + 64);
-    f16x8 cD0 = *(const f16x8*)(wB + 98304), cD1 = *(const f16x8*)(wB + 98304 + 64);
-#pragma unroll 4
-    for (int u = 0; u < 16; ++u) {
-        int un = (u < 15) ? u + 1 : 15;
-        const char* Hb = wB + un * 2048;
-        f16x8 nA0 = *(const f16x8*)(Hb), nA1 = *(const f16x8*)(Hb + 64);
-        f16x8 nD0 = *(const f16x8*)(Hb + 98304), nD1 = *(const f16x8*)(Hb + 98304 + 64);
-#pragma unroll
-        for (int t = 0; t < 8; t++) {
-            f16x2 sp = *(const f16x2*)((const char*)sc1 + (rbase + t * 16 + (l & 15)) * 72 + u * 4);
-            f16x8 x0 = ha0[t] * sp[0], x1 = ha1[t] * sp[0];
-            MFMA(accA[t], x0, cA0); MFMA(accA[t], x1, cA1);
-            x0 = ha0[t] * sp[1]; x1 = ha1[t] * sp[1];
-            MFMA(accA[t], x0, cD0); MFMA(accA[t], x1, cD1);
-        }
-        cA0 = nA0; cA1 = nA1; cD0 = nD0; cD1 = nD1;
-    }
-    int w = l & 15;
-#pragma unroll
-    for (int t = 0; t < 8; t++)
-#pragma unroll
-        for (int r = 0; r < 4; r++) {
-            int i = e0 + rbase + t * 16 + (l >> 4) * 4 + r;
-            tp_[(size_t)i * 16 + w] = (f16)(PW * accA[t][r]);
-        }
-}
-
-__global__ __launch_bounds__(256) void k_xfg(const float* __restrict__ h64f, const f16* __restrict__ tp1,
-                                             const int* __restrict__ rowptr,
-                                             float* __restrict__ xf,
-                                             const int* __restrict__ batchr, const int* __restrict__ batchp,
-                                             const float* __restrict__ w1, const float* __restrict__ b1,
-                                             const float* __restrict__ w2, const float* __restrict__ b2,
-                                             const float* __restrict__ w3, const float* __restrict__ b3,
-                                             float* __restrict__ out) {
-    __shared__ float xfs[64][17];
-    __shared__ float buck[64];
-    int tid = threadIdx.x;
-    if (tid < 64) buck[tid] = 0.f;
-    int mol = blockIdx.y;
-    float sign = mol ? 1.f : -1.f;
-    const int* batch = mol ? batchp : batchr;
-    const float* h_ = h64f + (size_t)mol * NN * 64;
-    const f16* tp = tp1 + (size_t)mol * NE * 16;
-    const int* rp = rowptr + mol * (NN + 1);
-    float* xf_ = xf + (size_t)mol * NN * 16;
-    int v = blockIdx.x * 64 + (tid >> 2), q = tid & 3;
-    int r0 = rp[v], r1 = rp[v + 1];
-    float a0 = 0.f, a1 = 0.f, a2 = 0.f, a3 = 0.f;
-    for (int i = r0; i < r1; i++) {
-        f16x4 t4 = *(const f16x4*)(tp + (size_t)i * 16 + q * 4);
-        a0 += (float)t4[0]; a1 += (float)t4[1]; a2 += (float)t4[2]; a3 += (float)t4[3];
-    }
-    float rc = 1.0f / fmaxf((float)(r1 - r0), 1.0f);
-    float4 hv = *(const float4*)(h_ + (size_t)v * 64 + q * 4);
-    float4 xv4;
-    xv4.x = fmaf(a0, rc, hv.x); xv4.y = fmaf(a1, rc, hv.y);
-    xv4.z = fmaf(a2, rc, hv.z); xv4.w = fmaf(a3, rc, hv.w);
-    xfs[tid >> 2][q * 4 + 0] = xv4.x; xfs[tid >> 2][q * 4 + 1] = xv4.y;
-    xfs[tid >> 2][q * 4 + 2] = xv4.z; xfs[tid >> 2][q * 4 + 3] = xv4.w;
-    *(float4*)(xf_ + (size_t)v * 16 + q * 4) = xv4;
-    __syncthreads();
-    if (tid < 64) {
-        int v2 = blockIdx.x * 64 + tid;
-        float xv[16];
-#pragma unroll
-        for (int c = 0; c < 16; c++) xv[c] = xfs[tid][c];
-        float aa[32];
-#pragma unroll
-        for (int j = 0; j < 32; j++) aa[j] = b1[j];
-#pragma unroll
-        for (int i = 0; i < 16; i++)
-#pragma unroll
-            for (int j = 0; j < 32; j++) aa[j] = fmaf(xv[i], w1[i * 32 + j], aa[j]);
-#pragma unroll
-        for (int j = 0; j < 32; j++) aa[j] = fmaxf(aa[j], 0.f);
-        float bb[16];
-#pragma unroll
-        for (int j = 0; j < 16; j++) bb[j] = b2[j];
-#pragma unroll
-        for (int i = 0; i < 32; i++)
-#pragma unroll
-            for (int j = 0; j < 16; j++) bb[j] = fmaf(aa[i], w2[i * 16 + j], bb[j]);
-#pragma unroll
-        for (int j = 0; j < 16; j++) bb[j] = fmaxf(bb[j], 0.f);
-        float val = b3[0];
-#pragma unroll
-        for (int i = 0; i < 16; i++) val = fmaf(bb[i], w3[i], val);
-        atomicAdd(&buck[batch[v2]], val);
-    }
-    __syncthreads();
-    if (tid < 64) atomicAdd(&out[tid], sign * buck[tid]);
-}
-
-__global__ __launch_bounds__(256) void k_sedge(const int* __restrict__ eir, const int* __restrict__ eip,
-                                               const int* __restrict__ batchr, const int* __restrict__ batchp,
-                                               const float* __restrict__ sh1d, const float* __restrict__ xf,
-                                               const float* __restrict__ w1, const float* __restrict__ b1,
-                                               const float* __restrict__ w2, const float* __restrict__ b2,
-                                               const float* __restrict__ w3, const float* __restrict__ b3,
-                                               float* __restrict__ out) {
-    __shared__ float buck[64];
-    int tid = threadIdx.x;
-    if (tid < 64) buck[tid] = 0.f;
-    __syncthreads();
-    int mol = blockIdx.y;
-    float sign = mol ? 1.f : -1.f;
-    const int* ei = mol ? eip : eir;
-    const int* batch = mol ? batchp : batchr;
-    const float* sh_ = sh1d + (size_t)mol * NE * 4;
-    const float* xf_ = xf + (size_t)mol * NN * 16;
-    int e = blockIdx.x * 256 + tid;
-    int s = ei[e], d = ei[NE + e];
-    float dist = sh_[e * 4 + 3];
-    float in[64];
-#pragma unroll
-    for (int i = 0; i < 32; i++) {
-        float t = dist - (float)i * GSTEP;
-        in[i] = __expf(GCOEFF * t * t);
-    }
-#pragma unroll
-    for (int i = 0; i < 16; i++) in[32 + i] = xf_[s * 16 + i];
-#pragma unroll
-    for (int i = 0; i < 16; i++) in[48 + i] = xf_[d * 16 + i];
-    float a[16];
-#pragma unroll
-    for (int j = 0; j < 16; j++) a[j] = b1[j];
-#pragma unroll
-    for (int i = 0; i < 64; i++)
-#pragma unroll
-        for (int j = 0; j < 16; j++) a[j] = fmaf(in[i], w1[i * 16 + j], a[j]);
-#pragma unroll
-    for (int j = 0; j < 16; j++) a[j] = fmaxf(a[j], 0.f);
-    float bb[16];
-#pragma unroll
-    for (int j = 0; j < 16; j++) bb[j] = b2[j];
-#pragma unroll
-    for (int i = 0; i < 16; i++)
-#pragma unroll
-        for (int j = 0; j < 16; j++) bb[j] = fmaf(a[i], w2[i * 16 + j], bb[j]);
-#pragma unroll
-    for (int j = 0; j < 16; j++) bb[j] = fmaxf(bb[j], 0.f);
-    float val = b3[0];
-#pragma unroll
-    for (int i = 0; i < 16; i++) val = fmaf(bb[i], w3[i], val);
-    atomicAdd(&buck[batch[s]], val);
-    __syncthreads();
-    if (tid < 64) atomicAdd(&out[tid], sign * buck[tid]);
+                int i = e0 + rbase + t * 16 + (l >> 4) * 4 + r;
+                tp_[(size_t)i * 16 + w] = (f16)(PW * accA[t][r]);
+            }
+    }
+    gridbar(P.bar, 5);
+
+    {
+        float (*xfs)[17] = (float(*)[17])smem;
+        float* buck = (float*)(smem + 2304);
+        if (tid < 64) buck[tid] = 0.f;
+        int mol = bid >> 8;
+        float sign = mol ? 1.f : -1.f;
+        const int* batch = mol ? P.batchp : P.batchr;
+        const float* h_ = P.h64f + (size_t)mol * NN * 64;
+        const f16* tp = P.tp1 + (size_t)mol * NE * 16;
+        const int* rp = P.rowptr + mol * (NN + 1);
+        float* xf_ = P.xf + (size_t)mol * NN * 16;
+        int v = (bid & 255) * 32 + (tid >> 2), q = tid & 3;
+        int r0 = rp[v], r1 = rp[v + 1];
+        float a0 = 0.f, a1 = 0.f, a2 = 0.f, a3 = 0.f;
+        for (int i = r0; i < r1; i++) {
+            f16x4 t4 = *(const f16x4*)(tp + (size_t)i * 16 + q * 4);
+            a0 += (float)t4[0]; a1 += (float)t4[1]; a2 += (float)t4[2]; a3 += (float)t4[3];
+        }
+        float rc = 1.0f / fmaxf((float)(r1 - r0), 1.0f);
+        float4 hv = *(const float4*)(h_ + (size_t)v * 64 + q * 4);
+        float4 xv4;
+        xv4.x = fmaf(a0, rc, hv.x); xv4.y = fmaf(a1, rc, hv.y);
+        xv4.z = fmaf(a2, rc, hv.z); xv4.w = fmaf(a3, rc, hv.w);
+        xfs[tid >> 2][q * 4 + 0] = xv4.x; xfs[tid >> 2][q * 4 + 1] = xv4.y;
+        xfs[tid >> 2][q * 4 + 2] = xv4.z; xfs[tid >> 2][q * 4 + 3] = xv4.w;
+        *(float4*)(xf_ + (size_t)v * 16 + q * 4) = xv4;
+        __syncthreads();
+        if (tid < 32) {
+            int v2 = (bid & 255) * 32 + tid;
+            float xv[16];
+#pragma unroll
+            for (int c = 0; c < 16; c++) xv[c] = xfs[tid][c];
+            float aa[32];
+#pragma unroll
+            for (int j = 0; j < 32; j++) aa[j] = P.snb1[j];
+#pragma unroll
+            for (int i = 0; i < 16; i++)
+#pragma unroll
+                for (int j = 0; j < 32; j++) aa[j] = fmaf(xv[i], P.snw1[i * 32 + j], aa[j]);
+#pragma unroll
+            for (int j = 0; j < 32; j++) aa[j] = fmaxf(aa[j], 0.f);
+            float bb[16];
+#pragma unroll
+            for (int j = 0; j < 16; j++) bb[j] = P.snb2[j];
+#pragma unroll
+            for (int i = 0; i < 32; i++)
+#pragma unroll
+                for (int j = 0; j < 16; j++) bb[j] = fmaf(aa[i], P.snw2[i * 16 + j], bb[j]);
+#pragma unroll
+            for (int j = 0; j < 16; j++) bb[j] = fmaxf(bb[j], 0.f);
+            float val = P.snb3[0];
+#pragma unroll
+            for (int i = 0; i < 16; i++) val = fmaf(bb[i], P.snw3[i], val);
+            atomicAdd(&buck[batch[v2]], val);
+        }
+        __syncthreads();
+        if (tid < 64) atomicAdd(&P.out[tid], sign * buck[tid]);
+    }
+    gridbar(P.bar, 6);
+
+    {
+        float* buck = (float*)smem;
+        if (tid < 64) buck[tid] = 0.f;
+        __syncthreads();
+#pragma unroll 1
+        for (int mol = 0; mol < 2; ++mol) {
+            float sign = mol ? 1.f : -1.f;
+            const int* ei = mol ? P.eip : P.eir;
+            const int* batch = mol ? P.batchp : P.batchr;
+            const float* sh_ = P.sh1d + (size_t)mol * NE * 4;
+            const float* xf_ = P.xf + (size_t)mol * NN * 16;
+            int e = gtid;
+            int s = ei[e], d = ei[NE + e];
+            float dist = sh_[e * 4 + 3];
+            float in[64];
+#pragma unroll
+            for (int i = 0; i < 32; i++) {
+                float t = dist - (float)i * GSTEP;
+                in[i] = __expf(GCOEFF * t * t);
+            }
+#pragma unroll
+            for (int i = 0; i < 16; i++) in[32 + i] = xf_[s * 16 + i];
+#pragma unroll
+            for (int i = 0; i < 16; i++) in[48 + i] = xf_[d * 16 + i];
+            float a[16];
+#pragma unroll
+            for (int j = 0; j < 16; j++) a[j] = P.seb1[j];
+#pragma unroll
+            for (int i = 0; i < 64; i++)
+#pragma unroll
+                for (int j = 0; j < 16; j++) a[j] = fmaf(in[i], P.sew1[i * 16 + j], a[j]);
+#pragma unroll
+            for (int j = 0; j < 16; j++) a[j] = fmaxf(a[j], 0.f);
+            float bb[16];
+#pragma unroll
+            for (int j = 0; j < 16; j++) bb[j] = P.seb2[j];
+#pragma unroll
+            for (int i = 0; i < 16; i++)
+#pragma unroll
+                for (int j = 0; j < 16; j++) bb[j] = fmaf(a[i], P.sew2[i * 16 + j], bb[j]);
+#pragma unroll
+            for (int j = 0; j < 16; j++) bb[j] = fmaxf(bb[j], 0.f);
+            float val = P.seb3[0];
+#pragma unroll
+            for (int i = 0; i < 16; i++) val = fmaf(bb[i], P.sew3[i], val);
+            atomicAdd(&buck[batch[s]], sign * val);
+        }
+        __syncthreads();
+        if (tid < 64) atomicAdd(&P.out[tid], buck[tid]);
+    }
 }
 
 extern "C" void kernel_launch(void* const* d_in, const int* in_sizes, int n_in,
                               void* d_out, int out_size, void* d_ws, size_t ws_size,
                               hipStream_t stream) {
-    const float* x_r = (const float*)d_in[0];
-    const float* pos_r = (const float*)d_in[1];
-    const int* ei_r = (const int*)d_in[2];
-    const int* batch_r = (const int*)d_in[3];
-    const float* x_p = (const float*)d_in[4];
-    const float* pos_p = (const float*)d_in[5];
-    const int* ei_p = (const int*)d_in[6];
-    const int* batch_p = (const int*)d_in[7];
-    const float* ne_w1 = (const float*)d_in[8];
-    const float* ne_b1 = (const float*)d_in[9];
-    const float* ne_w2 = (const float*)d_in[10];
-    const float* ne_b2 = (const float*)d_in[11];
-    const float* ee_w1 = (const float*)d_in[12];
-    const float* ee_b1 = (const float*)d_in[13];
-    const float* ee_w2 = (const float*)d_in[14];
-    const float* ee_b2 = (const float*)d_in[15];
-    const float* c0_w1 = (const float*)d_in[16];
-    const float* c0_b1 = (const float*)d_in[17];
-    const float* c0_w2 = (const float*)d_in[18];
-    const float* c0_b2 = (const float*)d_in[19];
-    const float* c1_w1 = (const float*)d_in[20];
-    const float* c1_b1 = (const float*)d_in[21];
-    const float* c1_w2 = (const float*)d_in[22];
-    const float* c1_b2 = (const float*)d_in[23];
-    const float* sn_w1 = (const float*)d_in[24];
-    const float* sn_b1 = (const float*)d_in[25];
-    const float* sn_w2 = (const float*)d_in[26];
-    const float* sn_b2 = (const float*)d_in[27];
-    const float* sn_w3 = (const float*)d_in[28];
-    const float* sn_b3 = (const float*)d_in[29];
-    const float* se_w1 = (const float*)d_in[30];
-    const float* se_b1 = (const float*)d_in[31];
-    const float* se_w2 = (const float*)d_in[32];
-    const float* se_b2 = (const float*)d_in[33];
-    const float* se_w3 = (const float*)d_in[34];
-    const float* se_b3 = (const float*)d_in[35];
-    float* out = (float*)d_out;
+    KP kp;
+    kp.xr = (const float*)d_in[0];
+    kp.posr = (const float*)d_in[1];
+    kp.eir = (const int*)d_in[2];
+    kp.batchr = (const int*)d_in[3];
+    kp.xp = (const float*)d_in[4];
+    kp.posp = (const float*)d_in[5];
+    kp.eip = (const int*)d_in[6];
+    kp.batchp = (const int*)d_in[7];
+    kp.nw1 = (const float*)d_in[8];
+    kp.nb1 = (const float*)d_in[9];
+    kp.nw2 = (const float*)d_in[10];
+    kp.nb2 = (const float*)d_in[11];
+    kp.ew1 = (const float*)d_in[12];
+    kp.eb1 = (const float*)d_in[13];
+    kp.ew2 = (const float*)d_in[14];
+    kp.eb2 = (const float*)d_in[15];
+    kp.c0w1 = (const float*)d_in[16];
+    kp.c0b1 = (const float*)d_in[17];
+    kp.c0w2 = (const float*)d_in[18];
+    kp.c0b2 = (const float*)d_in[19];
+    kp.c1w1 = (const float*)d_in[20];
+    kp.c1b1 = (const float*)d_in[21];
+    kp.c1w2 = (const float*)d_in[22];
+    kp.c1b2 = (const float*)d_in[23];
+    kp.snw1 = (const float*)d_in[24];
+    kp.snb1 = (const float*)d_in[25];
+    kp.snw2 = (const float*)d_in[26];
+    kp.snb2 = (const float*)d_in[27];
+    kp.snw3 = (const float*)d_in[28];
+    kp.snb3 = (const float*)d_in[29];
+    kp.sew1 = (const float*)d_in[30];
+    kp.seb1 = (const float*)d_in[31];
+    kp.sew2 = (const float*)d_in[32];
+    kp.seb2 = (const float*)d_in[33];
+    kp.sew3 = (const float*)d_in[34];
+    kp.seb3 = (const float*)d_in[35];
+    kp.out = (float*)d_out;
 
     char* p = (char*)d_ws;
     auto alloc = [&](size_t bytes) { char* r = p; p += (bytes + 255) & ~(size_t)255; return r; };
-    f16* w2t1 = (f16*)alloc(1280 * 64 * 2);
-    f16* w2t0 = (f16*)alloc(512 * 64 * 2);
-    f16* w1c0 = (f16*)alloc(48 * 64 * 2);
-    f16* w1c1 = (f16*)alloc(48 * 64 * 2);
-    f16* eemb16 = (f16*)alloc((size_t)2 * NE * 16 * 2);
-    f16* h16_16 = (f16*)alloc((size_t)2 * NN * 16 * 2);
-    f16* h64_16 = (f16*)alloc((size_t)2 * NN * 16 * 2);
-    float* h16f = (float*)alloc((size_t)2 * NN * 16 * 4);
-    float* sh1d = (float*)alloc((size_t)2 * NE * 4 * 4);
-    int* cntI = (int*)alloc((size_t)2 * NN * 4);
-    int* rowptr = (int*)alloc((size_t)2 * (NN + 1) * 4);
-    int* eord = (int*)alloc((size_t)2 * NE * 4);
-    f16* tp0 = (f16*)alloc((size_t)2 * NE * 64 * 2);
-    f16* tp1 = tp0;
-    float* h64f = (float*)alloc((size_t)2 * NN * 64 * 4);
-    float* xf = (float*)alloc((size_t)2 * NN * 16 * 4);
+    kp.w2t1 = (f16*)alloc(1280 * 64 * 2);
+    kp.w2t0 = (f16*)alloc(512 * 64 * 2);
+    kp.w1c0 = (f16*)alloc(48 * 64 * 2);
+    kp.w1c1 = (f16*)alloc(48 * 64 * 2);
+    kp.eemb16 = (f16*)alloc((size_t)2 * NE * 16 * 2);
+    kp.h16_16 = (f16*)alloc((size_t)2 * NN * 16 * 2);
+    kp.h64_16 = (f16*)alloc((size_t)2 * NN * 16 * 2);
+    kp.h16f = (float*)alloc((size_t)2 * NN * 16 * 4);
+    kp.sh1d = (float*)alloc((size_t)2 * NE * 4 * 4);
+    kp.cnt = (int*)alloc((size_t)2 * NN * 4);
+    kp.bar = (int*)alloc(256);
+    kp.rowptr = (int*)alloc((size_t)2 * (NN + 1) * 4);
+    kp.eord = (int*)alloc((size_t)2 * NE * 4);
+    kp.tp0 = (f16*)alloc((size_t)2 * NE * 64 * 2);
+    kp.tp1 = kp.tp0;
+    kp.h64f = (float*)alloc((size_t)2 * NN * 64 * 4);
+    kp.xf = (float*)alloc((size_t)2 * NN * 16 * 4);
     (void)ws_size; (void)n_in; (void)in_sizes; (void)out_size;
 
-    hipMemsetAsync(cntI, 0, (size_t)2 * NN * 4, stream);
-
-    dim3 blk256(256, 1, 1), blk128(128, 1, 1);
-    dim3 ge(NE / 256, 2, 1);
-    dim3 gc(NE / 256, 2, 1);
-
-    k_pre<<<dim3(896, 1, 1), blk256, 0, stream>>>(c0_w1, c0_b1, c1_w1, c1_b1, c0_w2, c0_b2, c1_w2, c1_b2,
-                                                  w1c0, w1c1, w2t0, w2t1,
-                                                  x_r, x_p, h16f, h16_16, ne_w1, ne_b1, ne_w2, ne_b2,
-                                                  ei_r, ei_p, pos_r, pos_p, sh1d, eemb16, cntI,
-                                                  ee_w1, ee_b1, ee_w2, ee_b2);
-    k_scan<<<dim3(2, 1, 1), blk256, 0, stream>>>(cntI, rowptr, out);
-    k_fill<<<ge, blk256, 0, stream>>>(ei_r, ei_p, rowptr, cntI, eord);
-    k_conv0<<<gc, blk128, 0, stream>>>(ei_r, ei_p, eord, eemb16, h16_16, sh1d, w1c0, w2t0, tp0);
-    k_up0g<<<dim3(NN / 64, 2, 1), blk256, 0, stream>>>(h16f, tp0, rowptr, h64f, h64_16);
-    k_conv1<<<gc, blk128, 0, stream>>>(ei_r, ei_p, eord, eemb16, h64_16, h64f, sh1d, w1c1, w2t1, tp1);
-    k_xfg<<<dim3(NN / 64, 2, 1), blk256, 0, stream>>>(h64f, tp1, rowptr, xf, batch_r, batch_p,
-                                                      sn_w1, sn_b1, sn_w2, sn_b2, sn_w3, sn_b3, out);
-    k_sedge<<<ge, blk256, 0, stream>>>(ei_r, ei_p, batch_r, batch_p, sh1d, xf,
-                                       se_w1, se_b1, se_w2, se_b2, se_w3, se_b3, out);
+    hipMemsetAsync(kp.cnt, 0, (size_t)2 * NN * 4 + 256, stream);
+
+    k_mega<<<dim3(NB, 1, 1), dim3(128, 1, 1), 0, stream>>>(kp);
 }
```
